# Kernel optimization log

Hardware: AMD Instinct MI355X
Metric: run time of the kernel (lower is better)

Reference implementation:

```python
import jax, jax.numpy as jnp
import numpy as np

N_SP, N_SPAT = 20000, 10000
E_SS, E_BIP, E_SP = 160000, 320000, 320000
H, C = 4, 64  # GAT heads / per-head channels (hidden_channels=64, concat=False)
EPS = 1e-6


def _gat(xs, xd, row, col, ea, Ws, Wd, a_s, a_d, a_e, We, b, num_dst, heads, ch, self_loops, concat):
    # PyG GATConv with edge_dim: linear -> per-head additive attention -> softmax over incoming edges -> scatter-add
    hs = (xs @ Ws).reshape(-1, heads, ch)          # [Ns,H,C]
    hd = (xd @ Wd).reshape(-1, heads, ch)          # [Nd,H,C]
    al_s = jnp.sum(hs * a_s, -1)                   # [Ns,H]
    al_d = jnp.sum(hd * a_d, -1)                   # [Nd,H]
    if self_loops:
        # add_self_loops with fill_value='mean': loop edge_attr = mean of incoming edge_attr per node
        cnt = jax.ops.segment_sum(jnp.ones((row.shape[0],), ea.dtype), col, num_dst)
        loop_ea = jax.ops.segment_sum(ea, col, num_dst) / jnp.maximum(cnt, 1.0)[:, None]
        loops = jnp.arange(num_dst, dtype=row.dtype)
        row = jnp.concatenate([row, loops])
        col = jnp.concatenate([col, loops])
        ea = jnp.concatenate([ea, loop_ea], 0)
    he = (ea @ We).reshape(-1, heads, ch)          # [E,H,C]
    al = jax.nn.leaky_relu(al_s[row] + al_d[col] + jnp.sum(he * a_e, -1), 0.2)  # [E,H]
    m = jax.ops.segment_max(al, col, num_segments=num_dst)
    ex = jnp.exp(al - m[col])
    den = jax.ops.segment_sum(ex, col, num_segments=num_dst)
    alpha = ex / (den[col] + 1e-16)
    out = jax.ops.segment_sum(hs[row] * alpha[..., None], col, num_segments=num_dst)  # [Nd,H,C]
    out = out.reshape(num_dst, heads * ch) if concat else out.mean(1)
    return out + b


def setup_inputs() -> dict:
    key = jax.random.key(0)
    ks = iter(jax.random.split(key, 64))
    f = lambda shape: jax.random.normal(next(ks), shape, jnp.float32)
    w = lambda shape: f(shape) / np.sqrt(shape[0])
    inp = {}
    inp['species_x_mean'] = f((N_SP, 32))
    inp['species_x_std'] = jax.random.uniform(next(ks), (N_SP, 32), jnp.float32)
    inp['traits_nanmask'] = jax.random.bernoulli(next(ks), 0.4, (N_SP, 32))
    inp['species_x_gen'] = f((N_SP, 64))
    inp['species_x_phylo'] = f((N_SP, 128))
    inp['spatial_x'] = f((N_SPAT, 12))
    inp['spatial_global_data'] = f((N_SPAT, 4))
    ei = lambda e, ns, nd: jnp.stack([jax.random.randint(next(ks), (e,), 0, ns, jnp.int32),
                                      jax.random.randint(next(ks), (e,), 0, nd, jnp.int32)])
    inp['ss_edge_index'] = ei(E_SS, N_SPAT, N_SPAT)
    inp['ss_edge_attr'] = jax.random.uniform(next(ks), (E_SS, 1), jnp.float32)
    inp['bip_edge_index'] = ei(E_BIP, N_SPAT, N_SP)
    inp['bip_edge_attr'] = jax.random.uniform(next(ks), (E_BIP, 1), jnp.float32)
    inp['sp_edge_index'] = ei(E_SP, N_SP, N_SP)
    inp['sp_edge_attr'] = jax.random.uniform(next(ks), (E_SP, 1), jnp.float32)
    # GAT conv params: space_gnn (sg0, sg1), species_gnn (pg0, pg1)
    for nm, din in [('sg0', 16), ('sg1', 64), ('pg0', 128), ('pg1', 64)]:
        inp[nm + '_W'] = w((din, H * C))
        inp[nm + '_as'] = f((H, C)) * 0.1
        inp[nm + '_ad'] = f((H, C)) * 0.1
        inp[nm + '_ae'] = f((H, C)) * 0.1
        inp[nm + '_We'] = w((1, H * C))
        inp[nm + '_b'] = jnp.zeros((C,), jnp.float32)
    # bipartite GATConv: heads=1, concat=True, src dim=hidden=64, dst dim=in_gen+in_phylo=192
    inp['bp_Ws'] = w((64, 64))
    inp['bp_Wd'] = w((192, 64))
    inp['bp_as'] = f((1, 64)) * 0.1
    inp['bp_ad'] = f((1, 64)) * 0.1
    inp['bp_ae'] = f((1, 64)) * 0.1
    inp['bp_We'] = w((1, 64))
    inp['bp_b'] = jnp.zeros((64,), jnp.float32)
    inp['sl_W'] = w((288, 64))
    inp['sl_b'] = jnp.zeros((64,), jnp.float32)
    inp['fc_W'] = w((64, 64))
    inp['fc_b'] = jnp.zeros((64,), jnp.float32)
    return inp


def reference(species_x_mean, species_x_std, traits_nanmask, species_x_gen, species_x_phylo,
              spatial_x, spatial_global_data, ss_edge_index, ss_edge_attr, bip_edge_index,
              bip_edge_attr, sp_edge_index, sp_edge_attr,
              sg0_W, sg0_as, sg0_ad, sg0_ae, sg0_We, sg0_b,
              sg1_W, sg1_as, sg1_ad, sg1_ae, sg1_We, sg1_b,
              pg0_W, pg0_as, pg0_ad, pg0_ae, pg0_We, pg0_b,
              pg1_W, pg1_as, pg1_ad, pg1_ae, pg1_We, pg1_b,
              bp_Ws, bp_Wd, bp_as, bp_ad, bp_ae, bp_We, bp_b,
              sl_W, sl_b, fc_W, fc_b):
    # inference path: no trait masking -> visibility = observed mask
    vis = (~traits_nanmask).astype(jnp.float32)
    sp_in = jnp.concatenate([species_x_mean, species_x_std, vis, species_x_gen, species_x_phylo], 1)
    sp_in = jax.nn.relu(sp_in @ sl_W + sl_b)                      # [N_SP,64]
    # spatial GNN (2 GATConv layers, heads=4, concat=False, self loops)
    h = jnp.concatenate([spatial_x, spatial_global_data], 1)      # [N_SPAT,16]
    r, c = ss_edge_index[0], ss_edge_index[1]
    h = jax.nn.relu(_gat(h, h, r, c, ss_edge_attr, sg0_W, sg0_W, sg0_as, sg0_ad, sg0_ae, sg0_We, sg0_b, N_SPAT, H, C, True, False))
    h = jax.nn.relu(_gat(h, h, r, c, ss_edge_attr, sg1_W, sg1_W, sg1_as, sg1_ad, sg1_ae, sg1_We, sg1_b, N_SPAT, H, C, True, False))
    # bipartite spatial->species GATConv (heads=1, concat=True, no self loops)
    part = jnp.concatenate([species_x_gen, species_x_phylo], 1)   # [N_SP,192]
    br, bc = bip_edge_index[0], bip_edge_index[1]
    sts = jax.nn.relu(_gat(h, part, br, bc, bip_edge_attr, bp_Ws, bp_Wd, bp_as, bp_ad, bp_ae, bp_We, bp_b, N_SP, 1, 64, False, True))
    # species GNN (2 GATConv layers)
    x = jnp.concatenate([sts, sp_in], 1)                          # [N_SP,128]
    pr, pc = sp_edge_index[0], sp_edge_index[1]
    x = jax.nn.relu(_gat(x, x, pr, pc, sp_edge_attr, pg0_W, pg0_W, pg0_as, pg0_ad, pg0_ae, pg0_We, pg0_b, N_SP, H, C, True, False))
    x = jax.nn.relu(_gat(x, x, pr, pc, sp_edge_attr, pg1_W, pg1_W, pg1_as, pg1_ad, pg1_ae, pg1_We, pg1_b, N_SP, H, C, True, False))
    ms = x @ fc_W + fc_b                                          # [N_SP, 2*out]
    mean, log_std = jnp.split(ms, 2, axis=-1)
    std = jax.nn.softplus(log_std) + EPS
    return mean, std
```

## Files before the change

kernel.cpp:

```cpp
#include <hip/hip_runtime.h>
#include <hip/hip_bf16.h>

#define NSP   20000
#define NSPAT 10000
#define ESS   160000
#define EBIP  320000
#define ESP   320000

static inline int cdiv_host(long a, long b) { return (int)((a + b - 1) / b); }

__device__ __forceinline__ float wave_red_sum(float p) {
#pragma unroll
  for (int m = 32; m >= 1; m >>= 1) p += __shfl_xor(p, m, 64);
  return p;
}

__device__ __forceinline__ float bf2f(unsigned short u) {
  return __uint_as_float(((unsigned int)u) << 16);
}
__device__ __forceinline__ unsigned short f2bf(float f) {
  unsigned int u = __float_as_uint(f);
  unsigned int r = (u + 0x7FFF + ((u >> 16) & 1)) >> 16;
  return (unsigned short)r;
}

__global__ void count3_kernel(
    const int* c1, int E1, int* cp1, int* rnk1, int n1,
    const int* c2, int E2, int* cp2, int* rnk2, int n2,
    const int* c3, int E3, int* cp3, int* rnk3, int n3,
    const unsigned int* __restrict__ mask, int* __restrict__ flag) {
  int b = blockIdx.x, t = threadIdx.x;
  if (b == gridDim.x - 1) {
    if (t < 64) {
      unsigned int w0 = mask[t], w1 = mask[t + 64], w2 = mask[t + 128], w3 = mask[t + 192];
      bool ai = (w0 <= 1u) && (w1 <= 1u) && (w2 <= 1u) && (w3 <= 1u);
      auto okf = [](unsigned int w) { return w == 0u || w == 0x3f800000u; };
      bool af = okf(w0) && okf(w1) && okf(w2) && okf(w3);
      unsigned long long bi = __ballot(ai), bf = __ballot(af);
      if (t == 0) *flag = (bi == ~0ull) ? 0 : ((bf == ~0ull) ? 2 : 1);
    }
    return;
  }
  int i = b * 256 + t;
  int total = E1 + E2 + E3;
  if (i >= total) return;
  int p = (i >> 8) & 7;
  if (i < E1) {
    int d = c1[i]; rnk1[i] = atomicAdd(&cp1[p * n1 + d], 1);
  } else if (i < E1 + E2) {
    int j = i - E1;
    int d = c2[j]; rnk2[j] = atomicAdd(&cp2[p * n2 + d], 1);
  } else {
    int j = i - E1 - E2;
    int d = c3[j]; rnk3[j] = atomicAdd(&cp3[p * n3 + d], 1);
  }
}

__global__ void merge3_kernel(int* cp1, int* c1, int n1,
                              int* cp2, int* c2, int n2,
                              int* cp3, int* c3, int n3) {
  int i = blockIdx.x * blockDim.x + threadIdx.x;
  int total = n1 + n2 + n3;
  if (i >= total) return;
  int *cp, *c; int n, d;
  if (i < n1) { cp = cp1; c = c1; n = n1; d = i; }
  else if (i < n1 + n2) { cp = cp2; c = c2; n = n2; d = i - n1; }
  else { cp = cp3; c = c3; n = n3; d = i - n1 - n2; }
  int s = 0;
#pragma unroll
  for (int p = 0; p < 8; ++p) { int t = cp[p * n + d]; cp[p * n + d] = s; s += t; }
  c[d] = s;
}

__global__ __launch_bounds__(1024) void scan3_kernel(
    const int* cntA, int nA, int* ptrA,
    const int* cntB, int nB, int* ptrB,
    const int* cntC, int nC, int* ptrC) {
  const int* cnt; int n; int* ptr;
  if (blockIdx.x == 0) { cnt = cntA; n = nA; ptr = ptrA; }
  else if (blockIdx.x == 1) { cnt = cntB; n = nB; ptr = ptrB; }
  else { cnt = cntC; n = nC; ptr = ptrC; }
  __shared__ int part[1024];
  int t = threadIdx.x;
  int ch = (n + 1023) / 1024;
  int beg = t * ch, end = min(beg + ch, n);
  int s = 0;
  for (int i = beg; i < end; ++i) s += cnt[i];
  part[t] = s;
  __syncthreads();
  for (int off = 1; off < 1024; off <<= 1) {
    int v = (t >= off) ? part[t - off] : 0;
    __syncthreads();
    part[t] += v;
    __syncthreads();
  }
  int run = (t == 0) ? 0 : part[t - 1];
  for (int i = beg; i < end; ++i) { ptr[i] = run; run += cnt[i]; }
  if (t == 1023) ptr[n] = part[1023];
}

__global__ void scatter3_kernel(
    const int* r1, const int* c1, const float* e1, int E1, const int* p1, const int* cp1, const int* k1, int n1, int* s1, float* a1,
    const int* r2, const int* c2, const float* e2, int E2, const int* p2, const int* cp2, const int* k2, int n2, int* s2, float* a2,
    const int* r3, const int* c3, const float* e3, int E3, const int* p3, const int* cp3, const int* k3, int n3, int* s3, float* a3) {
  int total = E1 + E2 + E3;
  for (int i = blockIdx.x * blockDim.x + threadIdx.x; i < total; i += gridDim.x * blockDim.x) {
    int p = (i >> 8) & 7;
    if (i < E1) {
      int d = c1[i];
      int pos = p1[d] + cp1[p * n1 + d] + k1[i];
      s1[pos] = r1[i]; a1[pos] = e1[i];
    } else if (i < E1 + E2) {
      int j = i - E1;
      int d = c2[j];
      int pos = p2[d] + cp2[p * n2 + d] + k2[j];
      s2[pos] = r2[j]; a2[pos] = e2[j];
    } else {
      int j = i - E1 - E2;
      int d = c3[j];
      int pos = p3[d] + cp3[p * n3 + d] + k3[j];
      s3[pos] = r3[j]; a3[pos] = e3[j];
    }
  }
}

__global__ void misc_kernel(
    const int* __restrict__ ss_ptr, const float* __restrict__ ss_cea, float* __restrict__ ss_lea,
    const int* __restrict__ pp_ptr, const float* __restrict__ pp_cea, float* __restrict__ pp_lea,
    const float* __restrict__ We0, const float* __restrict__ ae0,
    const float* __restrict__ We1, const float* __restrict__ ae1,
    const float* __restrict__ Web, const float* __restrict__ aeb,
    const float* __restrict__ We2, const float* __restrict__ ae2,
    const float* __restrict__ We3, const float* __restrict__ ae3,
    float* __restrict__ dotes,
    const float* __restrict__ mean, const float* __restrict__ stdv,
    const void* __restrict__ mask, const int* __restrict__ flag,
    const float* __restrict__ sx, const float* __restrict__ sg,
    float* __restrict__ spc96, float* __restrict__ h0) {
  int b = blockIdx.x, t = threadIdx.x;
  if (b < 118) {
    int i = b * 256 + t;
    if (i >= NSPAT + NSP) return;
    const int* ptr; const float* cea; float* lea; int d;
    if (i < NSPAT) { ptr = ss_ptr; cea = ss_cea; lea = ss_lea; d = i; }
    else { ptr = pp_ptr; cea = pp_cea; lea = pp_lea; d = i - NSPAT; }
    int e0 = ptr[d], e1 = ptr[d + 1];
    float s = 0.f;
    for (int e = e0; e < e1; ++e) s += cea[e];
    lea[d] = s / (float)max(e1 - e0, 1);
  } else if (b < 123) {
    int lb = b - 118;
    const float *We, *ae; int n, off;
    switch (lb) {
      case 0: We = We0; ae = ae0; n = 256; off = 0; break;
      case 1: We = We1; ae = ae1; n = 256; off = 4; break;
      case 2: We = Web; ae = aeb; n = 64;  off = 8; break;
      case 3: We = We2; ae = ae2; n = 256; off = 12; break;
      default: We = We3; ae = ae3; n = 256; off = 16; break;
    }
    if (t < n) {
      float p = wave_red_sum(We[t] * ae[t]);
      if ((t & 63) == 0) dotes[off + (t >> 6)] = p;
    }
  } else {
    const long totA = (long)NSP * 96;
    const long totB = (long)NSPAT * 16;
    long i = (long)(b - 123) * 256 + t;
    if (i >= totA + totB) return;
    int mode = *flag;
    if (i < totA) {
      int n = (int)(i / 96), c = (int)(i % 96);
      float v;
      if (c < 32) v = mean[(long)n * 32 + c];
      else if (c < 64) v = stdv[(long)n * 32 + (c - 32)];
      else {
        long j = (long)n * 32 + (c - 64);
        int mv;
        if (mode == 0) mv = ((const int*)mask)[j];
        else if (mode == 2) mv = (((const float*)mask)[j] != 0.0f);
        else mv = (int)((const unsigned char*)mask)[j];
        v = mv ? 0.f : 1.f;
      }
      spc96[i] = v;
    } else {
      long k = i - totA;
      int n = (int)(k / 16), c = (int)(k % 16);
      h0[k] = (c < 12) ? sx[(long)n * 12 + c] : sg[(long)n * 4 + (c - 12)];
    }
  }
}

struct XSrc { const float* p[5]; int w[5]; int n; };
struct PJob {
  XSrc xs; int M, K;
  const float* W; const float* bias; int mode;
  const float* a_s; const float* a_d;
  float* al_s; float* al_d;
  float* Y; float* Y2;
};

__device__ __forceinline__ void proj64_body(const PJob& J, int bid,
                                            float* wl, float* xl) {
  constexpr int KC = 32;
  constexpr int BR = 32;
  constexpr int KCP = 36;
  int t = threadIdx.x;
  long row0 = (long)bid * BR;
  if (row0 >= J.M) return;
  int cg = t & 15, rg = t >> 4;
  int c0 = cg * 4;

  float acc[2][4];
#pragma unroll
  for (int r = 0; r < 2; ++r)
#pragma unroll
    for (int j = 0; j < 4; ++j) acc[r][j] = 0.f;

  for (int k0 = 0; k0 < J.K; k0 += KC) {
    int seg = 0; int base = 0;
    while (k0 >= base + J.xs.w[seg]) { base += J.xs.w[seg]; ++seg; }
    const float* Xp = J.xs.p[seg];
    int stride = J.xs.w[seg];
    int kloc = k0 - base;

    __syncthreads();
    {
      const float4* ws = (const float4*)(J.W + (long)k0 * 64);
      float4* wd = (float4*)wl;
      wd[t] = ws[t];
      wd[t + 256] = ws[t + 256];
    }
    {
      int r = t >> 3, kq = (t & 7) * 4;
      long rr = row0 + r; if (rr >= J.M) rr = J.M - 1;
      float4 v = *(const float4*)(Xp + rr * stride + kloc + kq);
      *(float4*)(xl + r * KCP + kq) = v;
    }
    __syncthreads();

    for (int kg = 0; kg < KC; kg += 4) {
      float4 w0 = *(const float4*)(wl + (kg + 0) * 64 + c0);
      float4 w1 = *(const float4*)(wl + (kg + 1) * 64 + c0);
      float4 w2 = *(const float4*)(wl + (kg + 2) * 64 + c0);
      float4 w3 = *(const float4*)(wl + (kg + 3) * 64 + c0);
#pragma unroll
      for (int r = 0; r < 2; ++r) {
        float4 xv = *(const float4*)(xl + (rg * 2 + r) * KCP + kg);
        acc[r][0] = fmaf(xv.x, w0.x, acc[r][0]);
        acc[r][1] = fmaf(xv.x, w0.y, acc[r][1]);
        acc[r][2] = fmaf(xv.x, w0.z, acc[r][2]);
        acc[r][3] = fmaf(xv.x, w0.w, acc[r][3]);
        acc[r][0] = fmaf(xv.y, w1.x, acc[r][0]);
        acc[r][1] = fmaf(xv.y, w1.y, acc[r][1]);
        acc[r][2] = fmaf(xv.y, w1.z, acc[r][2]);
        acc[r][3] = fmaf(xv.y, w1.w, acc[r][3]);
        acc[r][0] = fmaf(xv.z, w2.x, acc[r][0]);
        acc[r][1] = fmaf(xv.z, w2.y, acc[r][1]);
        acc[r][2] = fmaf(xv.z, w2.z, acc[r][2]);
        acc[r][3] = fmaf(xv.z, w2.w, acc[r][3]);
        acc[r][0] = fmaf(xv.w, w3.x, acc[r][0]);
        acc[r][1] = fmaf(xv.w, w3.y, acc[r][1]);
        acc[r][2] = fmaf(xv.w, w3.z, acc[r][2]);
        acc[r][3] = fmaf(xv.w, w3.w, acc[r][3]);
      }
    }
  }

  float4 bv = make_float4(0.f, 0.f, 0.f, 0.f);
  float4 asv = make_float4(0.f, 0.f, 0.f, 0.f);
  float4 adv = make_float4(0.f, 0.f, 0.f, 0.f);
  if (J.bias) bv = *(const float4*)(J.bias + c0);
  if (J.a_s) asv = *(const float4*)(J.a_s + c0);
  if (J.a_d) adv = *(const float4*)(J.a_d + c0);

#pragma unroll
  for (int r = 0; r < 2; ++r) {
    long m = row0 + rg * 2 + r;
    bool ok = m < J.M;
    float v0 = acc[r][0] + bv.x, v1 = acc[r][1] + bv.y;
    float v2 = acc[r][2] + bv.z, v3 = acc[r][3] + bv.w;
    if (J.mode == 1) {
      if (ok)
        *(float4*)(J.Y + m * 64 + c0) = make_float4(
            fmaxf(v0, 0.f), fmaxf(v1, 0.f), fmaxf(v2, 0.f), fmaxf(v3, 0.f));
    } else if (J.mode == 2) {
      if (ok) {
        if (c0 < 32) {
          *(float4*)(J.Y + m * 32 + c0) = make_float4(v0, v1, v2, v3);
        } else {
          float4 o;
          o.x = fmaxf(v0, 0.f) + log1pf(__expf(-fabsf(v0))) + 1e-6f;
          o.y = fmaxf(v1, 0.f) + log1pf(__expf(-fabsf(v1))) + 1e-6f;
          o.z = fmaxf(v2, 0.f) + log1pf(__expf(-fabsf(v2))) + 1e-6f;
          o.w = fmaxf(v3, 0.f) + log1pf(__expf(-fabsf(v3))) + 1e-6f;
          *(float4*)(J.Y2 + m * 32 + (c0 - 32)) = o;
        }
      }
    } else if (ok && J.Y) {
      *(float4*)(J.Y + m * 64 + c0) = make_float4(v0, v1, v2, v3);
    }
    if (J.a_s) {
      float s = acc[r][0] * asv.x + acc[r][1] * asv.y + acc[r][2] * asv.z + acc[r][3] * asv.w;
      s += __shfl_xor(s, 1); s += __shfl_xor(s, 2);
      s += __shfl_xor(s, 4); s += __shfl_xor(s, 8);
      if (ok && cg == 0) J.al_s[m] = s;
    }
    if (J.a_d) {
      float s = acc[r][0] * adv.x + acc[r][1] * adv.y + acc[r][2] * adv.z + acc[r][3] * adv.w;
      s += __shfl_xor(s, 1); s += __shfl_xor(s, 2);
      s += __shfl_xor(s, 4); s += __shfl_xor(s, 8);
      if (ok && cg == 0) J.al_d[m] = s;
    }
  }
}

__global__ __launch_bounds__(256) void proj64x2_kernel(PJob j0, PJob j1, int nb0) {
  __shared__ float wl[32 * 64];
  __shared__ float xl[32 * 36];
  if ((int)blockIdx.x < nb0) proj64_body(j0, blockIdx.x, wl, xl);
  else proj64_body(j1, blockIdx.x - nb0, wl, xl);
}

__global__ __launch_bounds__(256) void proj_kernel(
    XSrc xsrc, int M, int K,
    const float* __restrict__ W, const float* __restrict__ bias, int mode,
    const float* __restrict__ a_s, const float* __restrict__ a_d,
    float* __restrict__ al_s, float* __restrict__ al_d,
    float* __restrict__ Y, float* __restrict__ Y2) {
  constexpr int NOUT = 256;
  constexpr int KC = 32;
  constexpr int RPT = 8;
  constexpr int BR = 32;
  constexpr int KCP = 36;
  constexpr int H = 4;
  __shared__ float wl[KC * NOUT];
  __shared__ float xl[BR * KCP];

  int t = threadIdx.x;
  int cg = t & 63, rg = t >> 6;
  int c0 = cg * 4;
  long row0 = (long)blockIdx.x * BR;

  float acc[RPT][4];
#pragma unroll
  for (int r = 0; r < RPT; ++r)
#pragma unroll
    for (int j = 0; j < 4; ++j) acc[r][j] = 0.f;

  for (int k0 = 0; k0 < K; k0 += KC) {
    int kc = min(KC, K - k0);
    int seg = 0; int base = 0;
    while (k0 >= base + xsrc.w[seg]) { base += xsrc.w[seg]; ++seg; }
    const float* Xp = xsrc.p[seg];
    int stride = xsrc.w[seg];
    int kloc = k0 - base;

    __syncthreads();
    {
      const float4* wsrc = (const float4*)(W + (long)k0 * NOUT);
      float4* wdst = (float4*)wl;
      for (int i = t; i < (kc * NOUT) >> 2; i += 256) wdst[i] = wsrc[i];
    }
    for (int i = t; i < BR * 8; i += 256) {
      int r = i >> 3, kq = (i & 7) * 4;
      if (kq < kc) {
        long rr = row0 + r; if (rr >= M) rr = M - 1;
        float4 v = *(const float4*)(Xp + rr * stride + kloc + kq);
        *(float4*)(xl + r * KCP + kq) = v;
      }
    }
    __syncthreads();

    for (int kg = 0; kg < kc; kg += 4) {
      float4 w0 = *(const float4*)(wl + (kg + 0) * NOUT + c0);
      float4 w1 = *(const float4*)(wl + (kg + 1) * NOUT + c0);
      float4 w2 = *(const float4*)(wl + (kg + 2) * NOUT + c0);
      float4 w3 = *(const float4*)(wl + (kg + 3) * NOUT + c0);
      float4 xv[RPT];
#pragma unroll
      for (int r = 0; r < RPT; ++r)
        xv[r] = *(const float4*)(xl + (rg * RPT + r) * KCP + kg);
#pragma unroll
      for (int r = 0; r < RPT; ++r) {
        acc[r][0] = fmaf(xv[r].x, w0.x, acc[r][0]);
        acc[r][1] = fmaf(xv[r].x, w0.y, acc[r][1]);
        acc[r][2] = fmaf(xv[r].x, w0.z, acc[r][2]);
        acc[r][3] = fmaf(xv[r].x, w0.w, acc[r][3]);
        acc[r][0] = fmaf(xv[r].y, w1.x, acc[r][0]);
        acc[r][1] = fmaf(xv[r].y, w1.y, acc[r][1]);
        acc[r][2] = fmaf(xv[r].y, w1.z, acc[r][2]);
        acc[r][3] = fmaf(xv[r].y, w1.w, acc[r][3]);
        acc[r][0] = fmaf(xv[r].z, w2.x, acc[r][0]);
        acc[r][1] = fmaf(xv[r].z, w2.y, acc[r][1]);
        acc[r][2] = fmaf(xv[r].z, w2.z, acc[r][2]);
        acc[r][3] = fmaf(xv[r].z, w2.w, acc[r][3]);
        acc[r][0] = fmaf(xv[r].w, w3.x, acc[r][0]);
        acc[r][1] = fmaf(xv[r].w, w3.y, acc[r][1]);
        acc[r][2] = fmaf(xv[r].w, w3.z, acc[r][2]);
        acc[r][3] = fmaf(xv[r].w, w3.w, acc[r][3]);
      }
    }
  }

  float4 asv = make_float4(0.f, 0.f, 0.f, 0.f);
  float4 adv = make_float4(0.f, 0.f, 0.f, 0.f);
  if (a_s) asv = *(const float4*)(a_s + c0);
  if (a_d) adv = *(const float4*)(a_d + c0);

#pragma unroll
  for (int r = 0; r < RPT; ++r) {
    long m = row0 + (long)rg * RPT + r;
    bool ok = m < M;
    if (ok && mode == 3) {
      ushort4 o;
      o.x = f2bf(acc[r][0]); o.y = f2bf(acc[r][1]);
      o.z = f2bf(acc[r][2]); o.w = f2bf(acc[r][3]);
      *(ushort4*)((unsigned short*)Y + m * NOUT + c0) = o;
    }
    if (a_s) {
      float s = acc[r][0] * asv.x + acc[r][1] * asv.y + acc[r][2] * asv.z + acc[r][3] * asv.w;
      s += __shfl_xor(s, 1); s += __shfl_xor(s, 2);
      s += __shfl_xor(s, 4); s += __shfl_xor(s, 8);
      if (ok && (cg & 15) == 0) al_s[m * H + (c0 >> 6)] = s;
    }
    if (a_d) {
      float s = acc[r][0] * adv.x + acc[r][1] * adv.y + acc[r][2] * adv.z + acc[r][3] * adv.w;
      s += __shfl_xor(s, 1); s += __shfl_xor(s, 2);
      s += __shfl_xor(s, 4); s += __shfl_xor(s, 8);
      if (ok && (cg & 15) == 0) al_d[m * H + (c0 >> 6)] = s;
    }
  }
  (void)bias; (void)Y2;
}

__device__ __forceinline__ void fma4_bf(float4& a, float al, ushort4 u) {
  a.x = fmaf(al, bf2f(u.x), a.x); a.y = fmaf(al, bf2f(u.y), a.y);
  a.z = fmaf(al, bf2f(u.z), a.z); a.w = fmaf(al, bf2f(u.w), a.w);
}
__device__ __forceinline__ void scale4(float4& a, float s) {
  a.x *= s; a.y *= s; a.z *= s; a.w *= s;
}

template <bool SELFLOOP>
__global__ __launch_bounds__(256) void gat4_fused(
    int Nd, const int* __restrict__ dptr, const int* __restrict__ csr_src,
    const float* __restrict__ csr_ea, const float* __restrict__ al_s,
    const float* __restrict__ al_d, const float* __restrict__ dote,
    const float* __restrict__ loop_ea, const unsigned short* __restrict__ hs,
    const float* __restrict__ bias, float* __restrict__ out) {
  int wave = threadIdx.x >> 6, lane = threadIdx.x & 63;
  int n = blockIdx.x * 4 + wave;
  if (n >= Nd) return;
  int h = lane >> 4;
  float ald = al_d[(long)n * 4 + h];
  float de = dote[h];
  int e0 = dptr[n], e1 = dptr[n + 1];
  float m0 = -INFINITY, d0 = 0.f;
  float4 a0 = make_float4(0.f, 0.f, 0.f, 0.f);
  if (SELFLOOP) {
    float l = al_s[(long)n * 4 + h] + ald + loop_ea[n] * de;
    l = (l > 0.f) ? l : 0.2f * l;
    m0 = l; d0 = 1.f;
    ushort4 u = *(const ushort4*)(hs + (long)n * 256 + lane * 4);
    a0.x = bf2f(u.x); a0.y = bf2f(u.y); a0.z = bf2f(u.z); a0.w = bf2f(u.w);
  }
  float m1 = -INFINITY, d1 = 0.f;
  float4 a1 = make_float4(0.f, 0.f, 0.f, 0.f);
  int e = e0;
  for (; e + 2 <= e1; e += 2) {
    int s0 = csr_src[e], s1 = csr_src[e + 1];
    float l0 = al_s[(long)s0 * 4 + h] + ald + csr_ea[e] * de;
    float l1 = al_s[(long)s1 * 4 + h] + ald + csr_ea[e + 1] * de;
    l0 = (l0 > 0.f) ? l0 : 0.2f * l0;
    l1 = (l1 > 0.f) ? l1 : 0.2f * l1;
    ushort4 u0 = *(const ushort4*)(hs + (long)s0 * 256 + lane * 4);
    ushort4 u1 = *(const ushort4*)(hs + (long)s1 * 256 + lane * 4);
    if (l0 > m0) { float sc = __expf(m0 - l0); d0 *= sc; scale4(a0, sc); m0 = l0; }
    float ex0 = __expf(l0 - m0);
    d0 += ex0;
    fma4_bf(a0, ex0, u0);
    if (l1 > m1) { float sc = __expf(m1 - l1); d1 *= sc; scale4(a1, sc); m1 = l1; }
    float ex1 = __expf(l1 - m1);
    d1 += ex1;
    fma4_bf(a1, ex1, u1);
  }
  if (e < e1) {
    int s0 = csr_src[e];
    float l0 = al_s[(long)s0 * 4 + h] + ald + csr_ea[e] * de;
    l0 = (l0 > 0.f) ? l0 : 0.2f * l0;
    ushort4 u0 = *(const ushort4*)(hs + (long)s0 * 256 + lane * 4);
    if (l0 > m0) { float sc = __expf(m0 - l0); d0 *= sc; scale4(a0, sc); m0 = l0; }
    float ex0 = __expf(l0 - m0);
    d0 += ex0;
    fma4_bf(a0, ex0, u0);
  }
  if (m1 != -INFINITY) {
    float M = fmaxf(m0, m1);
    float sA = (m0 == -INFINITY) ? 0.f : __expf(m0 - M);
    float sB = __expf(m1 - M);
    d0 = d0 * sA + d1 * sB;
    a0.x = a0.x * sA + a1.x * sB; a0.y = a0.y * sA + a1.y * sB;
    a0.z = a0.z * sA + a1.z * sB; a0.w = a0.w * sA + a1.w * sB;
  }
  float inv = 1.f / (d0 + 1e-16f);
  scale4(a0, inv);
  a0.x += __shfl_xor(a0.x, 16); a0.y += __shfl_xor(a0.y, 16);
  a0.z += __shfl_xor(a0.z, 16); a0.w += __shfl_xor(a0.w, 16);
  a0.x += __shfl_xor(a0.x, 32); a0.y += __shfl_xor(a0.y, 32);
  a0.z += __shfl_xor(a0.z, 32); a0.w += __shfl_xor(a0.w, 32);
  if (lane < 16) {
    float4 b = *(const float4*)(bias + lane * 4);
    float4 o;
    o.x = fmaxf(a0.x * 0.25f + b.x, 0.f);
    o.y = fmaxf(a0.y * 0.25f + b.y, 0.f);
    o.z = fmaxf(a0.z * 0.25f + b.z, 0.f);
    o.w = fmaxf(a0.w * 0.25f + b.w, 0.f);
    *(float4*)(out + (long)n * 64 + lane * 4) = o;
  }
}

__global__ __launch_bounds__(256) void gat1_fused(
    int Nd, const int* __restrict__ dptr, const int* __restrict__ csr_src,
    const float* __restrict__ csr_ea, const float* __restrict__ al_s,
    const float* __restrict__ al_d, const float* __restrict__ dote,
    const float* __restrict__ hs, const float* __restrict__ bias,
    float* __restrict__ out) {
  int wave = threadIdx.x >> 6, lane = threadIdx.x & 63;
  int n = blockIdx.x * 4 + wave;
  if (n >= Nd) return;
  float ald = al_d[n];
  float de = dote[0];
  int e0 = dptr[n], e1 = dptr[n + 1];
  float m0 = -INFINITY, d0 = 0.f, acc0 = 0.f;
  float m1 = -INFINITY, d1 = 0.f, acc1 = 0.f;
  int e = e0;
  for (; e + 2 <= e1; e += 2) {
    int s0 = csr_src[e], s1 = csr_src[e + 1];
    float l0 = al_s[s0] + ald + csr_ea[e] * de;
    float l1 = al_s[s1] + ald + csr_ea[e + 1] * de;
    l0 = (l0 > 0.f) ? l0 : 0.2f * l0;
    l1 = (l1 > 0.f) ? l1 : 0.2f * l1;
    float h0 = hs[(long)s0 * 64 + lane];
    float h1 = hs[(long)s1 * 64 + lane];
    if (l0 > m0) { float sc = __expf(m0 - l0); d0 *= sc; acc0 *= sc; m0 = l0; }
    float ex0 = __expf(l0 - m0);
    d0 += ex0; acc0 = fmaf(ex0, h0, acc0);
    if (l1 > m1) { float sc = __expf(m1 - l1); d1 *= sc; acc1 *= sc; m1 = l1; }
    float ex1 = __expf(l1 - m1);
    d1 += ex1; acc1 = fmaf(ex1, h1, acc1);
  }
  if (e < e1) {
    int s0 = csr_src[e];
    float l0 = al_s[s0] + ald + csr_ea[e] * de;
    l0 = (l0 > 0.f) ? l0 : 0.2f * l0;
    float h0 = hs[(long)s0 * 64 + lane];
    if (l0 > m0) { float sc = __expf(m0 - l0); d0 *= sc; acc0 *= sc; m0 = l0; }
    float ex0 = __expf(l0 - m0);
    d0 += ex0; acc0 = fmaf(ex0, h0, acc0);
  }
  if (m1 != -INFINITY) {
    float M = fmaxf(m0, m1);
    float sA = (m0 == -INFINITY) ? 0.f : __expf(m0 - M);
    float sB = __expf(m1 - M);
    d0 = d0 * sA + d1 * sB;
    acc0 = acc0 * sA + acc1 * sB;
  }
  float o = acc0 / (d0 + 1e-16f);
  out[(long)n * 64 + lane] = fmaxf(o + bias[lane], 0.f);
}

extern "C" void kernel_launch(void* const* d_in, const int* in_sizes, int n_in,
                              void* d_out, int out_size, void* d_ws, size_t ws_size,
                              hipStream_t stream) {
  const float* sp_mean = (const float*)d_in[0];
  const float* sp_std  = (const float*)d_in[1];
  const void*  nanmask = d_in[2];
  const float* sp_gen  = (const float*)d_in[3];
  const float* sp_phy  = (const float*)d_in[4];
  const float* spat_x  = (const float*)d_in[5];
  const float* spat_g  = (const float*)d_in[6];
  const int*   ss_ei   = (const int*)d_in[7];
  const float* ss_ea   = (const float*)d_in[8];
  const int*   bip_ei  = (const int*)d_in[9];
  const float* bip_ea  = (const float*)d_in[10];
  const int*   sp_ei   = (const int*)d_in[11];
  const float* sp_ea   = (const float*)d_in[12];
  const float* sg0_W = (const float*)d_in[13]; const float* sg0_as = (const float*)d_in[14];
  const float* sg0_ad = (const float*)d_in[15]; const float* sg0_ae = (const float*)d_in[16];
  const float* sg0_We = (const float*)d_in[17]; const float* sg0_b = (const float*)d_in[18];
  const float* sg1_W = (const float*)d_in[19]; const float* sg1_as = (const float*)d_in[20];
  const float* sg1_ad = (const float*)d_in[21]; const float* sg1_ae = (const float*)d_in[22];
  const float* sg1_We = (const float*)d_in[23]; const float* sg1_b = (const float*)d_in[24];
  const float* pg0_W = (const float*)d_in[25]; const float* pg0_as = (const float*)d_in[26];
  const float* pg0_ad = (const float*)d_in[27]; const float* pg0_ae = (const float*)d_in[28];
  const float* pg0_We = (const float*)d_in[29]; const float* pg0_b = (const float*)d_in[30];
  const float* pg1_W = (const float*)d_in[31]; const float* pg1_as = (const float*)d_in[32];
  const float* pg1_ad = (const float*)d_in[33]; const float* pg1_ae = (const float*)d_in[34];
  const float* pg1_We = (const float*)d_in[35]; const float* pg1_b = (const float*)d_in[36];
  const float* bp_Ws = (const float*)d_in[37]; const float* bp_Wd = (const float*)d_in[38];
  const float* bp_as = (const float*)d_in[39]; const float* bp_ad = (const float*)d_in[40];
  const float* bp_ae = (const float*)d_in[41]; const float* bp_We = (const float*)d_in[42];
  const float* bp_b  = (const float*)d_in[43];
  const float* sl_W  = (const float*)d_in[44]; const float* sl_b  = (const float*)d_in[45];
  const float* fc_W  = (const float*)d_in[46]; const float* fc_b  = (const float*)d_in[47];

  char* wsb = (char*)d_ws;
  size_t off = 0;
  auto A = [&](size_t nbytes) -> void* {
    void* p = wsb + off;
    off += (nbytes + 255) & ~(size_t)255;
    return p;
  };
  int* ss_cp = (int*)A((size_t)8 * NSPAT * 4);
  int* bp_cp = (int*)A((size_t)8 * NSP * 4);
  int* pp_cp = (int*)A((size_t)8 * NSP * 4);
  size_t zbytes = off;
  int*   ss_cnt = (int*)A((NSPAT + 1) * 4);
  int*   bp_cnt = (int*)A((NSP + 1) * 4);
  int*   pp_cnt = (int*)A((NSP + 1) * 4);
  int*   flag  = (int*)A(4);
  float* dotes = (float*)A(5 * 4 * sizeof(float));
  float* alS   = (float*)A((size_t)NSP * 4 * 4);
  float* alD   = (float*)A((size_t)NSP * 4 * 4);
  float* alSb  = (float*)A((size_t)NSPAT * 4);
  float* alDb  = (float*)A((size_t)NSP * 4);
  float* spc96 = (float*)A((size_t)NSP * 96 * 4);
  float* sp_in = (float*)A((size_t)NSP * 64 * 4);
  float* h0    = (float*)A((size_t)NSPAT * 16 * 4);
  float* h_a   = (float*)A((size_t)NSPAT * 64 * 4);
  float* h_b   = (float*)A((size_t)NSPAT * 64 * 4);
  float* HS    = (float*)A((size_t)NSP * 256 * 4);
  float* sts   = (float*)A((size_t)NSP * 64 * 4);
  float* x1    = (float*)A((size_t)NSP * 64 * 4);
  int*   ss_ptr = (int*)A((NSPAT + 1) * 4);
  int*   ss_src = (int*)A((size_t)ESS * 4);
  float* ss_cea = (float*)A((size_t)ESS * 4);
  int*   ss_rnk = (int*)A((size_t)ESS * 4);
  float* ss_lea = (float*)A((size_t)NSPAT * 4);
  int*   bp_ptr = (int*)A((NSP + 1) * 4);
  int*   bp_src = (int*)A((size_t)EBIP * 4);
  float* bp_cea = (float*)A((size_t)EBIP * 4);
  int*   bp_rnk = (int*)A((size_t)EBIP * 4);
  int*   pp_ptr = (int*)A((NSP + 1) * 4);
  int*   pp_src = (int*)A((size_t)ESP * 4);
  float* pp_cea = (float*)A((size_t)ESP * 4);
  int*   pp_rnk = (int*)A((size_t)ESP * 4);
  float* pp_lea = (float*)A((size_t)NSP * 4);
  (void)ws_size; (void)in_sizes; (void)n_in; (void)out_size;

  const int TB = 256;
  hipMemsetAsync(wsb, 0, zbytes, stream);

  count3_kernel<<<cdiv_host(ESS + EBIP + ESP, TB) + 1, TB, 0, stream>>>(
      ss_ei + ESS, ESS, ss_cp, ss_rnk, NSPAT,
      bip_ei + EBIP, EBIP, bp_cp, bp_rnk, NSP,
      sp_ei + ESP, ESP, pp_cp, pp_rnk, NSP,
      (const unsigned int*)nanmask, flag);
  merge3_kernel<<<cdiv_host(NSPAT + NSP + NSP, TB), TB, 0, stream>>>(
      ss_cp, ss_cnt, NSPAT, bp_cp, bp_cnt, NSP, pp_cp, pp_cnt, NSP);
  scan3_kernel<<<3, 1024, 0, stream>>>(ss_cnt, NSPAT, ss_ptr, bp_cnt, NSP, bp_ptr, pp_cnt, NSP, pp_ptr);
  scatter3_kernel<<<cdiv_host(ESS + EBIP + ESP, TB), TB, 0, stream>>>(
      ss_ei, ss_ei + ESS, ss_ea, ESS, ss_ptr, ss_cp, ss_rnk, NSPAT, ss_src, ss_cea,
      bip_ei, bip_ei + EBIP, bip_ea, EBIP, bp_ptr, bp_cp, bp_rnk, NSP, bp_src, bp_cea,
      sp_ei, sp_ei + ESP, sp_ea, ESP, pp_ptr, pp_cp, pp_rnk, NSP, pp_src, pp_cea);

  misc_kernel<<<123 + cdiv_host((long)NSP * 96 + (long)NSPAT * 16, TB), TB, 0, stream>>>(
      ss_ptr, ss_cea, ss_lea, pp_ptr, pp_cea, pp_lea,
      sg0_We, sg0_ae, sg1_We, sg1_ae, bp_We, bp_ae, pg0_We, pg0_ae, pg1_We, pg1_ae,
      dotes, sp_mean, sp_std, nanmask, flag, spat_x, spat_g, spc96, h0);

  {
    PJob j0{}; j0.xs.p[0] = spc96; j0.xs.w[0] = 96; j0.xs.p[1] = sp_gen; j0.xs.w[1] = 64;
    j0.xs.p[2] = sp_phy; j0.xs.w[2] = 128; j0.xs.n = 3;
    j0.M = NSP; j0.K = 288; j0.W = sl_W; j0.bias = sl_b; j0.mode = 1; j0.Y = sp_in;
    PJob j1{}; j1.xs.p[0] = sp_gen; j1.xs.w[0] = 64; j1.xs.p[1] = sp_phy; j1.xs.w[1] = 128;
    j1.xs.n = 2;
    j1.M = NSP; j1.K = 192; j1.W = bp_Wd; j1.mode = 0; j1.a_d = bp_ad; j1.al_d = alDb;
    int nb0 = cdiv_host(NSP, 32);
    proj64x2_kernel<<<nb0 + cdiv_host(NSP, 32), TB, 0, stream>>>(j0, j1, nb0);
  }

  {
    XSrc xs{}; xs.p[0] = h0; xs.w[0] = 16; xs.n = 1;
    proj_kernel<<<cdiv_host(NSPAT, 32), TB, 0, stream>>>(xs, NSPAT, 16, sg0_W, nullptr, 3,
        sg0_as, sg0_ad, alS, alD, HS, nullptr);
  }
  gat4_fused<true><<<cdiv_host(NSPAT, 4), TB, 0, stream>>>(
      NSPAT, ss_ptr, ss_src, ss_cea, alS, alD, dotes + 0, ss_lea,
      (const unsigned short*)HS, sg0_b, h_a);
  {
    XSrc xs{}; xs.p[0] = h_a; xs.w[0] = 64; xs.n = 1;
    proj_kernel<<<cdiv_host(NSPAT, 32), TB, 0, stream>>>(xs, NSPAT, 64, sg1_W, nullptr, 3,
        sg1_as, sg1_ad, alS, alD, HS, nullptr);
  }
  gat4_fused<true><<<cdiv_host(NSPAT, 4), TB, 0, stream>>>(
      NSPAT, ss_ptr, ss_src, ss_cea, alS, alD, dotes + 4, ss_lea,
      (const unsigned short*)HS, sg1_b, h_b);

  {
    PJob j0{}; j0.xs.p[0] = h_b; j0.xs.w[0] = 64; j0.xs.n = 1;
    j0.M = NSPAT; j0.K = 64; j0.W = bp_Ws; j0.mode = 0;
    j0.a_s = bp_as; j0.al_s = alSb; j0.Y = h_a;
    int nb0 = cdiv_host(NSPAT, 32);
    proj64x2_kernel<<<nb0, TB, 0, stream>>>(j0, j0, nb0);
  }
  gat1_fused<<<cdiv_host(NSP, 4), TB, 0, stream>>>(
      NSP, bp_ptr, bp_src, bp_cea, alSb, alDb, dotes + 8, h_a, bp_b, sts);

  {
    XSrc xs{}; xs.p[0] = sts; xs.w[0] = 64; xs.p[1] = sp_in; xs.w[1] = 64; xs.n = 2;
    proj_kernel<<<cdiv_host(NSP, 32), TB, 0, stream>>>(xs, NSP, 128, pg0_W, nullptr, 3,
        pg0_as, pg0_ad, alS, alD, HS, nullptr);
  }
  gat4_fused<true><<<cdiv_host(NSP, 4), TB, 0, stream>>>(
      NSP, pp_ptr, pp_src, pp_cea, alS, alD, dotes + 12, pp_lea,
      (const unsigned short*)HS, pg0_b, x1);
  {
    XSrc xs{}; xs.p[0] = x1; xs.w[0] = 64; xs.n = 1;
    proj_kernel<<<cdiv_host(NSP, 32), TB, 0, stream>>>(xs, NSP, 64, pg1_W, nullptr, 3,
        pg1_as, pg1_ad, alS, alD, HS, nullptr);
  }
  gat4_fused<true><<<cdiv_host(NSP, 4), TB, 0, stream>>>(
      NSP, pp_ptr, pp_src, pp_cea, alS, alD, dotes + 16, pp_lea,
      (const unsigned short*)HS, pg1_b, sts);

  {
    PJob j0{}; j0.xs.p[0] = sts; j0.xs.w[0] = 64; j0.xs.n = 1;
    j0.M = NSP; j0.K = 64; j0.W = fc_W; j0.bias = fc_b; j0.mode = 2;
    j0.Y = (float*)d_out; j0.Y2 = (float*)d_out + (long)NSP * 32;
    int nb0 = cdiv_host(NSP, 32);
    proj64x2_kernel<<<nb0, TB, 0, stream>>>(j0, j0, nb0);
  }
}
```

Baseline: 498.3 us.

## Fuse all stages into one cooperative persistent kernel with grid syncs

Replaces the chain of about fifteen separate launches (memset, CSR build, misc prep, projections, GAT aggregations) with a single cooperative mega-kernel. It uses grid-stride loops per stage and cg grid.sync between dependent phases, and the grid is sized from occupancy times CU count. This targets launch overhead and inter-kernel gaps. In exchange, every phase now runs under the occupancy limits of the largest stage's registers and shared memory, and each grid-wide barrier has its own cost.

```diff
diff --git a/kernel.cpp b/kernel.cpp
--- a/kernel.cpp
+++ b/kernel.cpp
@@ -1,5 +1,8 @@
 #include <hip/hip_runtime.h>
 #include <hip/hip_bf16.h>
+#include <hip/hip_cooperative_groups.h>
+
+namespace cg = cooperative_groups;
 
 #define NSP   20000
 #define NSPAT 10000
@@ -14,7 +17,6 @@
   for (int m = 32; m >= 1; m >>= 1) p += __shfl_xor(p, m, 64);
   return p;
 }
-
 __device__ __forceinline__ float bf2f(unsigned short u) {
   return __uint_as_float(((unsigned int)u) << 16);
 }
@@ -24,192 +26,53 @@
   return (unsigned short)r;
 }
 
-__global__ void count3_kernel(
-    const int* c1, int E1, int* cp1, int* rnk1, int n1,
-    const int* c2, int E2, int* cp2, int* rnk2, int n2,
-    const int* c3, int E3, int* cp3, int* rnk3, int n3,
-    const unsigned int* __restrict__ mask, int* __restrict__ flag) {
-  int b = blockIdx.x, t = threadIdx.x;
-  if (b == gridDim.x - 1) {
-    if (t < 64) {
-      unsigned int w0 = mask[t], w1 = mask[t + 64], w2 = mask[t + 128], w3 = mask[t + 192];
-      bool ai = (w0 <= 1u) && (w1 <= 1u) && (w2 <= 1u) && (w3 <= 1u);
-      auto okf = [](unsigned int w) { return w == 0u || w == 0x3f800000u; };
-      bool af = okf(w0) && okf(w1) && okf(w2) && okf(w3);
-      unsigned long long bi = __ballot(ai), bf = __ballot(af);
-      if (t == 0) *flag = (bi == ~0ull) ? 0 : ((bf == ~0ull) ? 2 : 1);
-    }
-    return;
-  }
-  int i = b * 256 + t;
-  int total = E1 + E2 + E3;
-  if (i >= total) return;
-  int p = (i >> 8) & 7;
-  if (i < E1) {
-    int d = c1[i]; rnk1[i] = atomicAdd(&cp1[p * n1 + d], 1);
-  } else if (i < E1 + E2) {
-    int j = i - E1;
-    int d = c2[j]; rnk2[j] = atomicAdd(&cp2[p * n2 + d], 1);
-  } else {
-    int j = i - E1 - E2;
-    int d = c3[j]; rnk3[j] = atomicAdd(&cp3[p * n3 + d], 1);
-  }
-}
-
-__global__ void merge3_kernel(int* cp1, int* c1, int n1,
-                              int* cp2, int* c2, int n2,
-                              int* cp3, int* c3, int n3) {
-  int i = blockIdx.x * blockDim.x + threadIdx.x;
-  int total = n1 + n2 + n3;
-  if (i >= total) return;
-  int *cp, *c; int n, d;
-  if (i < n1) { cp = cp1; c = c1; n = n1; d = i; }
-  else if (i < n1 + n2) { cp = cp2; c = c2; n = n2; d = i - n1; }
-  else { cp = cp3; c = c3; n = n3; d = i - n1 - n2; }
-  int s = 0;
-#pragma unroll
-  for (int p = 0; p < 8; ++p) { int t = cp[p * n + d]; cp[p * n + d] = s; s += t; }
-  c[d] = s;
-}
-
-__global__ __launch_bounds__(1024) void scan3_kernel(
-    const int* cntA, int nA, int* ptrA,
-    const int* cntB, int nB, int* ptrB,
-    const int* cntC, int nC, int* ptrC) {
-  const int* cnt; int n; int* ptr;
-  if (blockIdx.x == 0) { cnt = cntA; n = nA; ptr = ptrA; }
-  else if (blockIdx.x == 1) { cnt = cntB; n = nB; ptr = ptrB; }
-  else { cnt = cntC; n = nC; ptr = ptrC; }
-  __shared__ int part[1024];
-  int t = threadIdx.x;
-  int ch = (n + 1023) / 1024;
-  int beg = t * ch, end = min(beg + ch, n);
-  int s = 0;
-  for (int i = beg; i < end; ++i) s += cnt[i];
-  part[t] = s;
-  __syncthreads();
-  for (int off = 1; off < 1024; off <<= 1) {
-    int v = (t >= off) ? part[t - off] : 0;
-    __syncthreads();
-    part[t] += v;
-    __syncthreads();
-  }
-  int run = (t == 0) ? 0 : part[t - 1];
-  for (int i = beg; i < end; ++i) { ptr[i] = run; run += cnt[i]; }
-  if (t == 1023) ptr[n] = part[1023];
-}
-
-__global__ void scatter3_kernel(
-    const int* r1, const int* c1, const float* e1, int E1, const int* p1, const int* cp1, const int* k1, int n1, int* s1, float* a1,
-    const int* r2, const int* c2, const float* e2, int E2, const int* p2, const int* cp2, const int* k2, int n2, int* s2, float* a2,
-    const int* r3, const int* c3, const float* e3, int E3, const int* p3, const int* cp3, const int* k3, int n3, int* s3, float* a3) {
-  int total = E1 + E2 + E3;
-  for (int i = blockIdx.x * blockDim.x + threadIdx.x; i < total; i += gridDim.x * blockDim.x) {
-    int p = (i >> 8) & 7;
-    if (i < E1) {
-      int d = c1[i];
-      int pos = p1[d] + cp1[p * n1 + d] + k1[i];
-      s1[pos] = r1[i]; a1[pos] = e1[i];
-    } else if (i < E1 + E2) {
-      int j = i - E1;
-      int d = c2[j];
-      int pos = p2[d] + cp2[p * n2 + d] + k2[j];
-      s2[pos] = r2[j]; a2[pos] = e2[j];
-    } else {
-      int j = i - E1 - E2;
-      int d = c3[j];
-      int pos = p3[d] + cp3[p * n3 + d] + k3[j];
-      s3[pos] = r3[j]; a3[pos] = e3[j];
-    }
-  }
-}
-
-__global__ void misc_kernel(
-    const int* __restrict__ ss_ptr, const float* __restrict__ ss_cea, float* __restrict__ ss_lea,
-    const int* __restrict__ pp_ptr, const float* __restrict__ pp_cea, float* __restrict__ pp_lea,
-    const float* __restrict__ We0, const float* __restrict__ ae0,
-    const float* __restrict__ We1, const float* __restrict__ ae1,
-    const float* __restrict__ Web, const float* __restrict__ aeb,
-    const float* __restrict__ We2, const float* __restrict__ ae2,
-    const float* __restrict__ We3, const float* __restrict__ ae3,
-    float* __restrict__ dotes,
-    const float* __restrict__ mean, const float* __restrict__ stdv,
-    const void* __restrict__ mask, const int* __restrict__ flag,
-    const float* __restrict__ sx, const float* __restrict__ sg,
-    float* __restrict__ spc96, float* __restrict__ h0) {
-  int b = blockIdx.x, t = threadIdx.x;
-  if (b < 118) {
-    int i = b * 256 + t;
-    if (i >= NSPAT + NSP) return;
-    const int* ptr; const float* cea; float* lea; int d;
-    if (i < NSPAT) { ptr = ss_ptr; cea = ss_cea; lea = ss_lea; d = i; }
-    else { ptr = pp_ptr; cea = pp_cea; lea = pp_lea; d = i - NSPAT; }
-    int e0 = ptr[d], e1 = ptr[d + 1];
-    float s = 0.f;
-    for (int e = e0; e < e1; ++e) s += cea[e];
-    lea[d] = s / (float)max(e1 - e0, 1);
-  } else if (b < 123) {
-    int lb = b - 118;
-    const float *We, *ae; int n, off;
-    switch (lb) {
-      case 0: We = We0; ae = ae0; n = 256; off = 0; break;
-      case 1: We = We1; ae = ae1; n = 256; off = 4; break;
-      case 2: We = Web; ae = aeb; n = 64;  off = 8; break;
-      case 3: We = We2; ae = ae2; n = 256; off = 12; break;
-      default: We = We3; ae = ae3; n = 256; off = 16; break;
-    }
-    if (t < n) {
-      float p = wave_red_sum(We[t] * ae[t]);
-      if ((t & 63) == 0) dotes[off + (t >> 6)] = p;
-    }
-  } else {
-    const long totA = (long)NSP * 96;
-    const long totB = (long)NSPAT * 16;
-    long i = (long)(b - 123) * 256 + t;
-    if (i >= totA + totB) return;
-    int mode = *flag;
-    if (i < totA) {
-      int n = (int)(i / 96), c = (int)(i % 96);
-      float v;
-      if (c < 32) v = mean[(long)n * 32 + c];
-      else if (c < 64) v = stdv[(long)n * 32 + (c - 32)];
-      else {
-        long j = (long)n * 32 + (c - 64);
-        int mv;
-        if (mode == 0) mv = ((const int*)mask)[j];
-        else if (mode == 2) mv = (((const float*)mask)[j] != 0.0f);
-        else mv = (int)((const unsigned char*)mask)[j];
-        v = mv ? 0.f : 1.f;
-      }
-      spc96[i] = v;
-    } else {
-      long k = i - totA;
-      int n = (int)(k / 16), c = (int)(k % 16);
-      h0[k] = (c < 12) ? sx[(long)n * 12 + c] : sg[(long)n * 4 + (c - 12)];
-    }
-  }
-}
-
 struct XSrc { const float* p[5]; int w[5]; int n; };
-struct PJob {
+struct P64 {
   XSrc xs; int M, K;
   const float* W; const float* bias; int mode;
   const float* a_s; const float* a_d;
   float* al_s; float* al_d;
   float* Y; float* Y2;
 };
-
-__device__ __forceinline__ void proj64_body(const PJob& J, int bid,
-                                            float* wl, float* xl) {
-  constexpr int KC = 32;
-  constexpr int BR = 32;
-  constexpr int KCP = 36;
+struct P256 {
+  XSrc xs; int M, K;
+  const float* W;
+  const float* a_s; const float* a_d;
+  float* al_s; float* al_d;
+  unsigned short* Y;
+};
+
+struct MegaArgs {
+  uint4* zbase; int zwords;
+  const int *ss_row, *ss_col; const float* ss_eaI;
+  const int *bp_row, *bp_col; const float* bp_eaI;
+  const int *pp_row, *pp_col; const float* pp_eaI;
+  int *ss_cp, *bp_cp, *pp_cp;
+  int *ss_rnk, *bp_rnk, *pp_rnk;
+  int *ss_cnt, *bp_cnt, *pp_cnt;
+  int *ss_ptr, *bp_ptr, *pp_ptr;
+  int *ss_src; float* ss_cea;
+  int *bp_src; float* bp_cea;
+  int *pp_src; float* pp_cea;
+  float *ss_lea, *pp_lea;
+  const unsigned int* mask; int* flag;
+  const float* We[5]; const float* ae[5]; float* dotes;
+  const float* mean; const float* stdv; const float* sx; const float* sgd;
+  float* spc96; float* h0;
+  P64 sl, bpWd, bpWs, fc;
+  P256 sg0, sg1, pg0, pg1;
+  float *alS, *alD, *alSb, *alDb;
+  const unsigned short* HS;
+  const float *sg0_b, *sg1_b, *pg0_b, *pg1_b, *bp_b;
+  float *h_a, *h_b, *sts, *x1;
+};
+
+__device__ void proj64_tile(const P64& J, int bid, float* wl, float* xl) {
+  constexpr int KC = 32, BR = 32, KCP = 36;
   int t = threadIdx.x;
   long row0 = (long)bid * BR;
-  if (row0 >= J.M) return;
-  int cg = t & 15, rg = t >> 4;
-  int c0 = cg * 4;
-
+  int cg_ = t & 15, rg = t >> 4;
+  int c0 = cg_ * 4;
   float acc[2][4];
 #pragma unroll
   for (int r = 0; r < 2; ++r)
@@ -217,12 +80,11 @@
     for (int j = 0; j < 4; ++j) acc[r][j] = 0.f;
 
   for (int k0 = 0; k0 < J.K; k0 += KC) {
-    int seg = 0; int base = 0;
+    int seg = 0, base = 0;
     while (k0 >= base + J.xs.w[seg]) { base += J.xs.w[seg]; ++seg; }
     const float* Xp = J.xs.p[seg];
     int stride = J.xs.w[seg];
     int kloc = k0 - base;
-
     __syncthreads();
     {
       const float4* ws = (const float4*)(J.W + (long)k0 * 64);
@@ -237,7 +99,6 @@
       *(float4*)(xl + r * KCP + kq) = v;
     }
     __syncthreads();
-
     for (int kg = 0; kg < KC; kg += 4) {
       float4 w0 = *(const float4*)(wl + (kg + 0) * 64 + c0);
       float4 w1 = *(const float4*)(wl + (kg + 1) * 64 + c0);
@@ -303,134 +164,111 @@
       float s = acc[r][0] * asv.x + acc[r][1] * asv.y + acc[r][2] * asv.z + acc[r][3] * asv.w;
       s += __shfl_xor(s, 1); s += __shfl_xor(s, 2);
       s += __shfl_xor(s, 4); s += __shfl_xor(s, 8);
-      if (ok && cg == 0) J.al_s[m] = s;
+      if (ok && cg_ == 0) J.al_s[m] = s;
     }
     if (J.a_d) {
       float s = acc[r][0] * adv.x + acc[r][1] * adv.y + acc[r][2] * adv.z + acc[r][3] * adv.w;
       s += __shfl_xor(s, 1); s += __shfl_xor(s, 2);
       s += __shfl_xor(s, 4); s += __shfl_xor(s, 8);
-      if (ok && cg == 0) J.al_d[m] = s;
-    }
-  }
-}
-
-__global__ __launch_bounds__(256) void proj64x2_kernel(PJob j0, PJob j1, int nb0) {
-  __shared__ float wl[32 * 64];
-  __shared__ float xl[32 * 36];
-  if ((int)blockIdx.x < nb0) proj64_body(j0, blockIdx.x, wl, xl);
-  else proj64_body(j1, blockIdx.x - nb0, wl, xl);
-}
-
-__global__ __launch_bounds__(256) void proj_kernel(
-    XSrc xsrc, int M, int K,
-    const float* __restrict__ W, const float* __restrict__ bias, int mode,
-    const float* __restrict__ a_s, const float* __restrict__ a_d,
-    float* __restrict__ al_s, float* __restrict__ al_d,
-    float* __restrict__ Y, float* __restrict__ Y2) {
-  constexpr int NOUT = 256;
-  constexpr int KC = 32;
-  constexpr int RPT = 8;
-  constexpr int BR = 32;
-  constexpr int KCP = 36;
-  constexpr int H = 4;
-  __shared__ float wl[KC * NOUT];
-  __shared__ float xl[BR * KCP];
-
+      if (ok && cg_ == 0) J.al_d[m] = s;
+    }
+  }
+}
+
+__device__ void proj64_grid(const P64& J, float* wl, float* xl) {
+  int nb = (J.M + 31) >> 5;
+  for (int b = blockIdx.x; b < nb; b += gridDim.x) proj64_tile(J, b, wl, xl);
+}
+
+__device__ void proj256_grid(const P256& J, float* wl, float* xl) {
+  constexpr int KC = 32, RPT = 8, BR = 32, KCP = 36;
   int t = threadIdx.x;
-  int cg = t & 63, rg = t >> 6;
-  int c0 = cg * 4;
-  long row0 = (long)blockIdx.x * BR;
-
-  float acc[RPT][4];
-#pragma unroll
-  for (int r = 0; r < RPT; ++r)
-#pragma unroll
-    for (int j = 0; j < 4; ++j) acc[r][j] = 0.f;
-
-  for (int k0 = 0; k0 < K; k0 += KC) {
-    int kc = min(KC, K - k0);
-    int seg = 0; int base = 0;
-    while (k0 >= base + xsrc.w[seg]) { base += xsrc.w[seg]; ++seg; }
-    const float* Xp = xsrc.p[seg];
-    int stride = xsrc.w[seg];
-    int kloc = k0 - base;
-
-    __syncthreads();
-    {
-      const float4* wsrc = (const float4*)(W + (long)k0 * NOUT);
-      float4* wdst = (float4*)wl;
-      for (int i = t; i < (kc * NOUT) >> 2; i += 256) wdst[i] = wsrc[i];
-    }
-    for (int i = t; i < BR * 8; i += 256) {
-      int r = i >> 3, kq = (i & 7) * 4;
-      if (kq < kc) {
-        long rr = row0 + r; if (rr >= M) rr = M - 1;
-        float4 v = *(const float4*)(Xp + rr * stride + kloc + kq);
-        *(float4*)(xl + r * KCP + kq) = v;
+  int cg_ = t & 63, rg = t >> 6;
+  int c0 = cg_ * 4;
+  int nb = (J.M + 31) >> 5;
+  for (int b = blockIdx.x; b < nb; b += gridDim.x) {
+    long row0 = (long)b * BR;
+    float acc[RPT][4];
+#pragma unroll
+    for (int r = 0; r < RPT; ++r)
+#pragma unroll
+      for (int j = 0; j < 4; ++j) acc[r][j] = 0.f;
+
+    for (int k0 = 0; k0 < J.K; k0 += KC) {
+      int kc = min(KC, J.K - k0);
+      int seg = 0, base = 0;
+      while (k0 >= base + J.xs.w[seg]) { base += J.xs.w[seg]; ++seg; }
+      const float* Xp = J.xs.p[seg];
+      int stride = J.xs.w[seg];
+      int kloc = k0 - base;
+      __syncthreads();
+      {
+        const float4* wsrc = (const float4*)(J.W + (long)k0 * 256);
+        float4* wdst = (float4*)wl;
+        for (int i = t; i < (kc * 256) >> 2; i += 256) wdst[i] = wsrc[i];
       }
-    }
-    __syncthreads();
-
-    for (int kg = 0; kg < kc; kg += 4) {
-      float4 w0 = *(const float4*)(wl + (kg + 0) * NOUT + c0);
-      float4 w1 = *(const float4*)(wl + (kg + 1) * NOUT + c0);
-      float4 w2 = *(const float4*)(wl + (kg + 2) * NOUT + c0);
-      float4 w3 = *(const float4*)(wl + (kg + 3) * NOUT + c0);
-      float4 xv[RPT];
-#pragma unroll
-      for (int r = 0; r < RPT; ++r)
-        xv[r] = *(const float4*)(xl + (rg * RPT + r) * KCP + kg);
-#pragma unroll
-      for (int r = 0; r < RPT; ++r) {
-        acc[r][0] = fmaf(xv[r].x, w0.x, acc[r][0]);
-        acc[r][1] = fmaf(xv[r].x, w0.y, acc[r][1]);
-        acc[r][2] = fmaf(xv[r].x, w0.z, acc[r][2]);
-        acc[r][3] = fmaf(xv[r].x, w0.w, acc[r][3]);
-        acc[r][0] = fmaf(xv[r].y, w1.x, acc[r][0]);
-        acc[r][1] = fmaf(xv[r].y, w1.y, acc[r][1]);
-        acc[r][2] = fmaf(xv[r].y, w1.z, acc[r][2]);
-        acc[r][3] = fmaf(xv[r].y, w1.w, acc[r][3]);
-        acc[r][0] = fmaf(xv[r].z, w2.x, acc[r][0]);
-        acc[r][1] = fmaf(xv[r].z, w2.y, acc[r][1]);
-        acc[r][2] = fmaf(xv[r].z, w2.z, acc[r][2]);
-        acc[r][3] = fmaf(xv[r].z, w2.w, acc[r][3]);
-        acc[r][0] = fmaf(xv[r].w, w3.x, acc[r][0]);
-        acc[r][1] = fmaf(xv[r].w, w3.y, acc[r][1]);
-        acc[r][2] = fmaf(xv[r].w, w3.z, acc[r][2]);
-        acc[r][3] = fmaf(xv[r].w, w3.w, acc[r][3]);
+      for (int i = t; i < BR * 8; i += 256) {
+        int r = i >> 3, kq = (i & 7) * 4;
+        if (kq < kc) {
+          long rr = row0 + r; if (rr >= J.M) rr = J.M - 1;
+          float4 v = *(const float4*)(Xp + rr * stride + kloc + kq);
+          *(float4*)(xl + r * KCP + kq) = v;
+        }
       }
-    }
-  }
-
-  float4 asv = make_float4(0.f, 0.f, 0.f, 0.f);
-  float4 adv = make_float4(0.f, 0.f, 0.f, 0.f);
-  if (a_s) asv = *(const float4*)(a_s + c0);
-  if (a_d) adv = *(const float4*)(a_d + c0);
-
-#pragma unroll
-  for (int r = 0; r < RPT; ++r) {
-    long m = row0 + (long)rg * RPT + r;
-    bool ok = m < M;
-    if (ok && mode == 3) {
-      ushort4 o;
-      o.x = f2bf(acc[r][0]); o.y = f2bf(acc[r][1]);
-      o.z = f2bf(acc[r][2]); o.w = f2bf(acc[r][3]);
-      *(ushort4*)((unsigned short*)Y + m * NOUT + c0) = o;
-    }
-    if (a_s) {
+      __syncthreads();
+      for (int kg = 0; kg < kc; kg += 4) {
+        float4 w0 = *(const float4*)(wl + (kg + 0) * 256 + c0);
+        float4 w1 = *(const float4*)(wl + (kg + 1) * 256 + c0);
+        float4 w2 = *(const float4*)(wl + (kg + 2) * 256 + c0);
+        float4 w3 = *(const float4*)(wl + (kg + 3) * 256 + c0);
+        float4 xv[RPT];
+#pragma unroll
+        for (int r = 0; r < RPT; ++r)
+          xv[r] = *(const float4*)(xl + (rg * RPT + r) * KCP + kg);
+#pragma unroll
+        for (int r = 0; r < RPT; ++r) {
+          acc[r][0] = fmaf(xv[r].x, w0.x, acc[r][0]);
+          acc[r][1] = fmaf(xv[r].x, w0.y, acc[r][1]);
+          acc[r][2] = fmaf(xv[r].x, w0.z, acc[r][2]);
+          acc[r][3] = fmaf(xv[r].x, w0.w, acc[r][3]);
+          acc[r][0] = fmaf(xv[r].y, w1.x, acc[r][0]);
+          acc[r][1] = fmaf(xv[r].y, w1.y, acc[r][1]);
+          acc[r][2] = fmaf(xv[r].y, w1.z, acc[r][2]);
+          acc[r][3] = fmaf(xv[r].y, w1.w, acc[r][3]);
+          acc[r][0] = fmaf(xv[r].z, w2.x, acc[r][0]);
+          acc[r][1] = fmaf(xv[r].z, w2.y, acc[r][1]);
+          acc[r][2] = fmaf(xv[r].z, w2.z, acc[r][2]);
+          acc[r][3] = fmaf(xv[r].z, w2.w, acc[r][3]);
+          acc[r][0] = fmaf(xv[r].w, w3.x, acc[r][0]);
+          acc[r][1] = fmaf(xv[r].w, w3.y, acc[r][1]);
+          acc[r][2] = fmaf(xv[r].w, w3.z, acc[r][2]);
+          acc[r][3] = fmaf(xv[r].w, w3.w, acc[r][3]);
+        }
+      }
+    }
+
+    float4 asv = *(const float4*)(J.a_s + c0);
+    float4 adv = *(const float4*)(J.a_d + c0);
+#pragma unroll
+    for (int r = 0; r < RPT; ++r) {
+      long m = row0 + (long)rg * RPT + r;
+      bool ok = m < J.M;
+      if (ok) {
+        ushort4 o;
+        o.x = f2bf(acc[r][0]); o.y = f2bf(acc[r][1]);
+        o.z = f2bf(acc[r][2]); o.w = f2bf(acc[r][3]);
+        *(ushort4*)(J.Y + m * 256 + c0) = o;
+      }
       float s = acc[r][0] * asv.x + acc[r][1] * asv.y + acc[r][2] * asv.z + acc[r][3] * asv.w;
       s += __shfl_xor(s, 1); s += __shfl_xor(s, 2);
       s += __shfl_xor(s, 4); s += __shfl_xor(s, 8);
-      if (ok && (cg & 15) == 0) al_s[m * H + (c0 >> 6)] = s;
-    }
-    if (a_d) {
-      float s = acc[r][0] * adv.x + acc[r][1] * adv.y + acc[r][2] * adv.z + acc[r][3] * adv.w;
-      s += __shfl_xor(s, 1); s += __shfl_xor(s, 2);
-      s += __shfl_xor(s, 4); s += __shfl_xor(s, 8);
-      if (ok && (cg & 15) == 0) al_d[m * H + (c0 >> 6)] = s;
-    }
-  }
-  (void)bias; (void)Y2;
+      if (ok && (cg_ & 15) == 0) J.al_s[m * 4 + (c0 >> 6)] = s;
+      float d = acc[r][0] * adv.x + acc[r][1] * adv.y + acc[r][2] * adv.z + acc[r][3] * adv.w;
+      d += __shfl_xor(d, 1); d += __shfl_xor(d, 2);
+      d += __shfl_xor(d, 4); d += __shfl_xor(d, 8);
+      if (ok && (cg_ & 15) == 0) J.al_d[m * 4 + (c0 >> 6)] = d;
+    }
+  }
 }
 
 __device__ __forceinline__ void fma4_bf(float4& a, float al, ushort4 u) {
@@ -441,132 +279,312 @@
   a.x *= s; a.y *= s; a.z *= s; a.w *= s;
 }
 
-template <bool SELFLOOP>
-__global__ __launch_bounds__(256) void gat4_fused(
-    int Nd, const int* __restrict__ dptr, const int* __restrict__ csr_src,
-    const float* __restrict__ csr_ea, const float* __restrict__ al_s,
-    const float* __restrict__ al_d, const float* __restrict__ dote,
-    const float* __restrict__ loop_ea, const unsigned short* __restrict__ hs,
-    const float* __restrict__ bias, float* __restrict__ out) {
+__device__ void gat4_grid(int Nd, const int* dptr, const int* csr_src,
+                          const float* csr_ea, const float* al_s, const float* al_d,
+                          const float* dote, const float* loop_ea,
+                          const unsigned short* hs, const float* bias, float* out) {
   int wave = threadIdx.x >> 6, lane = threadIdx.x & 63;
-  int n = blockIdx.x * 4 + wave;
-  if (n >= Nd) return;
   int h = lane >> 4;
-  float ald = al_d[(long)n * 4 + h];
   float de = dote[h];
-  int e0 = dptr[n], e1 = dptr[n + 1];
-  float m0 = -INFINITY, d0 = 0.f;
-  float4 a0 = make_float4(0.f, 0.f, 0.f, 0.f);
-  if (SELFLOOP) {
+  for (int n = blockIdx.x * 4 + wave; n < Nd; n += gridDim.x * 4) {
+    float ald = al_d[(long)n * 4 + h];
+    int e0 = dptr[n], e1 = dptr[n + 1];
     float l = al_s[(long)n * 4 + h] + ald + loop_ea[n] * de;
     l = (l > 0.f) ? l : 0.2f * l;
-    m0 = l; d0 = 1.f;
-    ushort4 u = *(const ushort4*)(hs + (long)n * 256 + lane * 4);
-    a0.x = bf2f(u.x); a0.y = bf2f(u.y); a0.z = bf2f(u.z); a0.w = bf2f(u.w);
-  }
-  float m1 = -INFINITY, d1 = 0.f;
-  float4 a1 = make_float4(0.f, 0.f, 0.f, 0.f);
-  int e = e0;
-  for (; e + 2 <= e1; e += 2) {
-    int s0 = csr_src[e], s1 = csr_src[e + 1];
-    float l0 = al_s[(long)s0 * 4 + h] + ald + csr_ea[e] * de;
-    float l1 = al_s[(long)s1 * 4 + h] + ald + csr_ea[e + 1] * de;
-    l0 = (l0 > 0.f) ? l0 : 0.2f * l0;
-    l1 = (l1 > 0.f) ? l1 : 0.2f * l1;
-    ushort4 u0 = *(const ushort4*)(hs + (long)s0 * 256 + lane * 4);
-    ushort4 u1 = *(const ushort4*)(hs + (long)s1 * 256 + lane * 4);
-    if (l0 > m0) { float sc = __expf(m0 - l0); d0 *= sc; scale4(a0, sc); m0 = l0; }
-    float ex0 = __expf(l0 - m0);
-    d0 += ex0;
-    fma4_bf(a0, ex0, u0);
-    if (l1 > m1) { float sc = __expf(m1 - l1); d1 *= sc; scale4(a1, sc); m1 = l1; }
-    float ex1 = __expf(l1 - m1);
-    d1 += ex1;
-    fma4_bf(a1, ex1, u1);
-  }
-  if (e < e1) {
-    int s0 = csr_src[e];
-    float l0 = al_s[(long)s0 * 4 + h] + ald + csr_ea[e] * de;
-    l0 = (l0 > 0.f) ? l0 : 0.2f * l0;
-    ushort4 u0 = *(const ushort4*)(hs + (long)s0 * 256 + lane * 4);
-    if (l0 > m0) { float sc = __expf(m0 - l0); d0 *= sc; scale4(a0, sc); m0 = l0; }
-    float ex0 = __expf(l0 - m0);
-    d0 += ex0;
-    fma4_bf(a0, ex0, u0);
-  }
-  if (m1 != -INFINITY) {
-    float M = fmaxf(m0, m1);
-    float sA = (m0 == -INFINITY) ? 0.f : __expf(m0 - M);
-    float sB = __expf(m1 - M);
-    d0 = d0 * sA + d1 * sB;
-    a0.x = a0.x * sA + a1.x * sB; a0.y = a0.y * sA + a1.y * sB;
-    a0.z = a0.z * sA + a1.z * sB; a0.w = a0.w * sA + a1.w * sB;
-  }
-  float inv = 1.f / (d0 + 1e-16f);
-  scale4(a0, inv);
-  a0.x += __shfl_xor(a0.x, 16); a0.y += __shfl_xor(a0.y, 16);
-  a0.z += __shfl_xor(a0.z, 16); a0.w += __shfl_xor(a0.w, 16);
-  a0.x += __shfl_xor(a0.x, 32); a0.y += __shfl_xor(a0.y, 32);
-  a0.z += __shfl_xor(a0.z, 32); a0.w += __shfl_xor(a0.w, 32);
-  if (lane < 16) {
-    float4 b = *(const float4*)(bias + lane * 4);
-    float4 o;
-    o.x = fmaxf(a0.x * 0.25f + b.x, 0.f);
-    o.y = fmaxf(a0.y * 0.25f + b.y, 0.f);
-    o.z = fmaxf(a0.z * 0.25f + b.z, 0.f);
-    o.w = fmaxf(a0.w * 0.25f + b.w, 0.f);
-    *(float4*)(out + (long)n * 64 + lane * 4) = o;
-  }
-}
-
-__global__ __launch_bounds__(256) void gat1_fused(
-    int Nd, const int* __restrict__ dptr, const int* __restrict__ csr_src,
-    const float* __restrict__ csr_ea, const float* __restrict__ al_s,
-    const float* __restrict__ al_d, const float* __restrict__ dote,
-    const float* __restrict__ hs, const float* __restrict__ bias,
-    float* __restrict__ out) {
+    float m0 = l, d0 = 1.f;
+    float4 a0;
+    {
+      ushort4 u = *(const ushort4*)(hs + (long)n * 256 + lane * 4);
+      a0.x = bf2f(u.x); a0.y = bf2f(u.y); a0.z = bf2f(u.z); a0.w = bf2f(u.w);
+    }
+    float m1 = -INFINITY, d1 = 0.f;
+    float4 a1 = make_float4(0.f, 0.f, 0.f, 0.f);
+    int e = e0;
+    for (; e + 2 <= e1; e += 2) {
+      int s0 = csr_src[e], s1 = csr_src[e + 1];
+      float l0 = al_s[(long)s0 * 4 + h] + ald + csr_ea[e] * de;
+      float l1 = al_s[(long)s1 * 4 + h] + ald + csr_ea[e + 1] * de;
+      l0 = (l0 > 0.f) ? l0 : 0.2f * l0;
+      l1 = (l1 > 0.f) ? l1 : 0.2f * l1;
+      ushort4 u0 = *(const ushort4*)(hs + (long)s0 * 256 + lane * 4);
+      ushort4 u1 = *(const ushort4*)(hs + (long)s1 * 256 + lane * 4);
+      if (l0 > m0) { float sc = __expf(m0 - l0); d0 *= sc; scale4(a0, sc); m0 = l0; }
+      float ex0 = __expf(l0 - m0);
+      d0 += ex0;
+      fma4_bf(a0, ex0, u0);
+      if (l1 > m1) { float sc = __expf(m1 - l1); d1 *= sc; scale4(a1, sc); m1 = l1; }
+      float ex1 = __expf(l1 - m1);
+      d1 += ex1;
+      fma4_bf(a1, ex1, u1);
+    }
+    if (e < e1) {
+      int s0 = csr_src[e];
+      float l0 = al_s[(long)s0 * 4 + h] + ald + csr_ea[e] * de;
+      l0 = (l0 > 0.f) ? l0 : 0.2f * l0;
+      ushort4 u0 = *(const ushort4*)(hs + (long)s0 * 256 + lane * 4);
+      if (l0 > m0) { float sc = __expf(m0 - l0); d0 *= sc; scale4(a0, sc); m0 = l0; }
+      float ex0 = __expf(l0 - m0);
+      d0 += ex0;
+      fma4_bf(a0, ex0, u0);
+    }
+    if (m1 != -INFINITY) {
+      float M = fmaxf(m0, m1);
+      float sA = __expf(m0 - M);
+      float sB = __expf(m1 - M);
+      d0 = d0 * sA + d1 * sB;
+      a0.x = a0.x * sA + a1.x * sB; a0.y = a0.y * sA + a1.y * sB;
+      a0.z = a0.z * sA + a1.z * sB; a0.w = a0.w * sA + a1.w * sB;
+    }
+    float inv = 1.f / (d0 + 1e-16f);
+    scale4(a0, inv);
+    a0.x += __shfl_xor(a0.x, 16); a0.y += __shfl_xor(a0.y, 16);
+    a0.z += __shfl_xor(a0.z, 16); a0.w += __shfl_xor(a0.w, 16);
+    a0.x += __shfl_xor(a0.x, 32); a0.y += __shfl_xor(a0.y, 32);
+    a0.z += __shfl_xor(a0.z, 32); a0.w += __shfl_xor(a0.w, 32);
+    if (lane < 16) {
+      float4 b = *(const float4*)(bias + lane * 4);
+      float4 o;
+      o.x = fmaxf(a0.x * 0.25f + b.x, 0.f);
+      o.y = fmaxf(a0.y * 0.25f + b.y, 0.f);
+      o.z = fmaxf(a0.z * 0.25f + b.z, 0.f);
+      o.w = fmaxf(a0.w * 0.25f + b.w, 0.f);
+      *(float4*)(out + (long)n * 64 + lane * 4) = o;
+    }
+  }
+}
+
+__device__ void gat1_grid(int Nd, const int* dptr, const int* csr_src,
+                          const float* csr_ea, const float* al_s, const float* al_d,
+                          const float* dote, const float* hs, const float* bias,
+                          float* out) {
   int wave = threadIdx.x >> 6, lane = threadIdx.x & 63;
-  int n = blockIdx.x * 4 + wave;
-  if (n >= Nd) return;
-  float ald = al_d[n];
   float de = dote[0];
-  int e0 = dptr[n], e1 = dptr[n + 1];
-  float m0 = -INFINITY, d0 = 0.f, acc0 = 0.f;
-  float m1 = -INFINITY, d1 = 0.f, acc1 = 0.f;
-  int e = e0;
-  for (; e + 2 <= e1; e += 2) {
-    int s0 = csr_src[e], s1 = csr_src[e + 1];
-    float l0 = al_s[s0] + ald + csr_ea[e] * de;
-    float l1 = al_s[s1] + ald + csr_ea[e + 1] * de;
-    l0 = (l0 > 0.f) ? l0 : 0.2f * l0;
-    l1 = (l1 > 0.f) ? l1 : 0.2f * l1;
-    float h0 = hs[(long)s0 * 64 + lane];
-    float h1 = hs[(long)s1 * 64 + lane];
-    if (l0 > m0) { float sc = __expf(m0 - l0); d0 *= sc; acc0 *= sc; m0 = l0; }
-    float ex0 = __expf(l0 - m0);
-    d0 += ex0; acc0 = fmaf(ex0, h0, acc0);
-    if (l1 > m1) { float sc = __expf(m1 - l1); d1 *= sc; acc1 *= sc; m1 = l1; }
-    float ex1 = __expf(l1 - m1);
-    d1 += ex1; acc1 = fmaf(ex1, h1, acc1);
-  }
-  if (e < e1) {
-    int s0 = csr_src[e];
-    float l0 = al_s[s0] + ald + csr_ea[e] * de;
-    l0 = (l0 > 0.f) ? l0 : 0.2f * l0;
-    float h0 = hs[(long)s0 * 64 + lane];
-    if (l0 > m0) { float sc = __expf(m0 - l0); d0 *= sc; acc0 *= sc; m0 = l0; }
-    float ex0 = __expf(l0 - m0);
-    d0 += ex0; acc0 = fmaf(ex0, h0, acc0);
-  }
-  if (m1 != -INFINITY) {
-    float M = fmaxf(m0, m1);
-    float sA = (m0 == -INFINITY) ? 0.f : __expf(m0 - M);
-    float sB = __expf(m1 - M);
-    d0 = d0 * sA + d1 * sB;
-    acc0 = acc0 * sA + acc1 * sB;
-  }
-  float o = acc0 / (d0 + 1e-16f);
-  out[(long)n * 64 + lane] = fmaxf(o + bias[lane], 0.f);
+  for (int n = blockIdx.x * 4 + wave; n < Nd; n += gridDim.x * 4) {
+    float ald = al_d[n];
+    int e0 = dptr[n], e1 = dptr[n + 1];
+    float m0 = -INFINITY, d0 = 0.f, acc0 = 0.f;
+    float m1 = -INFINITY, d1 = 0.f, acc1 = 0.f;
+    int e = e0;
+    for (; e + 2 <= e1; e += 2) {
+      int s0 = csr_src[e], s1 = csr_src[e + 1];
+      float l0 = al_s[s0] + ald + csr_ea[e] * de;
+      float l1 = al_s[s1] + ald + csr_ea[e + 1] * de;
+      l0 = (l0 > 0.f) ? l0 : 0.2f * l0;
+      l1 = (l1 > 0.f) ? l1 : 0.2f * l1;
+      float h0 = hs[(long)s0 * 64 + lane];
+      float h1 = hs[(long)s1 * 64 + lane];
+      if (l0 > m0) { float sc = __expf(m0 - l0); d0 *= sc; acc0 *= sc; m0 = l0; }
+      float ex0 = __expf(l0 - m0);
+      d0 += ex0; acc0 = fmaf(ex0, h0, acc0);
+      if (l1 > m1) { float sc = __expf(m1 - l1); d1 *= sc; acc1 *= sc; m1 = l1; }
+      float ex1 = __expf(l1 - m1);
+      d1 += ex1; acc1 = fmaf(ex1, h1, acc1);
+    }
+    if (e < e1) {
+      int s0 = csr_src[e];
+      float l0 = al_s[s0] + ald + csr_ea[e] * de;
+      l0 = (l0 > 0.f) ? l0 : 0.2f * l0;
+      float h0 = hs[(long)s0 * 64 + lane];
+      if (l0 > m0) { float sc = __expf(m0 - l0); d0 *= sc; acc0 *= sc; m0 = l0; }
+      float ex0 = __expf(l0 - m0);
+      d0 += ex0; acc0 = fmaf(ex0, h0, acc0);
+    }
+    if (m1 != -INFINITY) {
+      float M = fmaxf(m0, m1);
+      float sA = (m0 == -INFINITY) ? 0.f : __expf(m0 - M);
+      float sB = __expf(m1 - M);
+      d0 = d0 * sA + d1 * sB;
+      acc0 = acc0 * sA + acc1 * sB;
+    }
+    float o = acc0 / (d0 + 1e-16f);
+    out[(long)n * 64 + lane] = fmaxf(o + bias[lane], 0.f);
+  }
+}
+
+__global__ __launch_bounds__(256, 4) void mega_kernel(MegaArgs A) {
+  __shared__ __align__(16) float smem[32 * 256 + 32 * 36];
+  float* wl = smem;
+  float* xl = smem + 32 * 256;
+  cg::grid_group g = cg::this_grid();
+  int t = threadIdx.x;
+  int gtid = blockIdx.x * 256 + t;
+  int gsz = gridDim.x * 256;
+
+  for (int i = gtid; i < A.zwords; i += gsz) A.zbase[i] = make_uint4(0, 0, 0, 0);
+  g.sync();
+
+  {
+    const int NB = (ESS + EBIP + ESP + 255) / 256;
+    for (int b = blockIdx.x; b < NB + 1; b += gridDim.x) {
+      if (b == NB) {
+        if (t < 64) {
+          unsigned int w0 = A.mask[t], w1 = A.mask[t + 64];
+          unsigned int w2 = A.mask[t + 128], w3 = A.mask[t + 192];
+          bool ai = (w0 <= 1u) && (w1 <= 1u) && (w2 <= 1u) && (w3 <= 1u);
+          bool af = (w0 == 0u || w0 == 0x3f800000u) && (w1 == 0u || w1 == 0x3f800000u) &&
+                    (w2 == 0u || w2 == 0x3f800000u) && (w3 == 0u || w3 == 0x3f800000u);
+          unsigned long long bi = __ballot(ai), bf = __ballot(af);
+          if (t == 0) *A.flag = (bi == ~0ull) ? 0 : ((bf == ~0ull) ? 2 : 1);
+        }
+      } else {
+        int i = b * 256 + t;
+        if (i < ESS + EBIP + ESP) {
+          int p = (i >> 8) & 7;
+          if (i < ESS) {
+            int d = A.ss_col[i]; A.ss_rnk[i] = atomicAdd(&A.ss_cp[p * NSPAT + d], 1);
+          } else if (i < ESS + EBIP) {
+            int j = i - ESS;
+            int d = A.bp_col[j]; A.bp_rnk[j] = atomicAdd(&A.bp_cp[p * NSP + d], 1);
+          } else {
+            int j = i - ESS - EBIP;
+            int d = A.pp_col[j]; A.pp_rnk[j] = atomicAdd(&A.pp_cp[p * NSP + d], 1);
+          }
+        }
+      }
+    }
+  }
+  g.sync();
+
+  for (int i = gtid; i < NSPAT + NSP + NSP; i += gsz) {
+    int *cp, *c; int n, d;
+    if (i < NSPAT) { cp = A.ss_cp; c = A.ss_cnt; n = NSPAT; d = i; }
+    else if (i < NSPAT + NSP) { cp = A.bp_cp; c = A.bp_cnt; n = NSP; d = i - NSPAT; }
+    else { cp = A.pp_cp; c = A.pp_cnt; n = NSP; d = i - NSPAT - NSP; }
+    int s = 0;
+#pragma unroll
+    for (int p = 0; p < 8; ++p) { int v = cp[p * n + d]; cp[p * n + d] = s; s += v; }
+    c[d] = s;
+  }
+  g.sync();
+
+  if (blockIdx.x < 3) {
+    const int* cnt; int n; int* ptr;
+    if (blockIdx.x == 0) { cnt = A.ss_cnt; n = NSPAT; ptr = A.ss_ptr; }
+    else if (blockIdx.x == 1) { cnt = A.bp_cnt; n = NSP; ptr = A.bp_ptr; }
+    else { cnt = A.pp_cnt; n = NSP; ptr = A.pp_ptr; }
+    int* part = (int*)smem;
+    int ch = (n + 255) / 256;
+    int beg = t * ch, end = min(beg + ch, n);
+    int s = 0;
+    for (int i = beg; i < end; ++i) s += cnt[i];
+    part[t] = s;
+    __syncthreads();
+    for (int off2 = 1; off2 < 256; off2 <<= 1) {
+      int v = (t >= off2) ? part[t - off2] : 0;
+      __syncthreads();
+      part[t] += v;
+      __syncthreads();
+    }
+    int run = (t == 0) ? 0 : part[t - 1];
+    for (int i = beg; i < end; ++i) { ptr[i] = run; run += cnt[i]; }
+    if (t == 255) ptr[n] = part[255];
+  }
+  g.sync();
+
+  for (int i = gtid; i < ESS + EBIP + ESP; i += gsz) {
+    int p = (i >> 8) & 7;
+    if (i < ESS) {
+      int d = A.ss_col[i];
+      int pos = A.ss_ptr[d] + A.ss_cp[p * NSPAT + d] + A.ss_rnk[i];
+      A.ss_src[pos] = A.ss_row[i]; A.ss_cea[pos] = A.ss_eaI[i];
+    } else if (i < ESS + EBIP) {
+      int j = i - ESS;
+      int d = A.bp_col[j];
+      int pos = A.bp_ptr[d] + A.bp_cp[p * NSP + d] + A.bp_rnk[j];
+      A.bp_src[pos] = A.bp_row[j]; A.bp_cea[pos] = A.bp_eaI[j];
+    } else {
+      int j = i - ESS - EBIP;
+      int d = A.pp_col[j];
+      int pos = A.pp_ptr[d] + A.pp_cp[p * NSP + d] + A.pp_rnk[j];
+      A.pp_src[pos] = A.pp_row[j]; A.pp_cea[pos] = A.pp_eaI[j];
+    }
+  }
+  g.sync();
+
+  {
+    const int NB_LEAF = (NSPAT + NSP + 255) / 256;
+    const long totA = (long)NSP * 96, totB = (long)NSPAT * 16;
+    const int NB_PREP = (int)((totA + totB + 255) / 256);
+    const int NBT = NB_LEAF + 5 + NB_PREP;
+    int mode = *A.flag;
+    for (int b = blockIdx.x; b < NBT; b += gridDim.x) {
+      if (b < NB_LEAF) {
+        int i = b * 256 + t;
+        if (i < NSPAT + NSP) {
+          const int* ptr; const float* cea; float* lea; int d;
+          if (i < NSPAT) { ptr = A.ss_ptr; cea = A.ss_cea; lea = A.ss_lea; d = i; }
+          else { ptr = A.pp_ptr; cea = A.pp_cea; lea = A.pp_lea; d = i - NSPAT; }
+          int e0 = ptr[d], e1 = ptr[d + 1];
+          float s = 0.f;
+          for (int e = e0; e < e1; ++e) s += cea[e];
+          lea[d] = s / (float)max(e1 - e0, 1);
+        }
+      } else if (b < NB_LEAF + 5) {
+        int lb = b - NB_LEAF;
+        int n = (lb == 2) ? 64 : 256;
+        int off2 = lb * 4;
+        if (t < n) {
+          float p = wave_red_sum(A.We[lb][t] * A.ae[lb][t]);
+          if ((t & 63) == 0) A.dotes[off2 + (t >> 6)] = p;
+        }
+      } else {
+        long i = (long)(b - NB_LEAF - 5) * 256 + t;
+        if (i < totA + totB) {
+          if (i < totA) {
+            int n = (int)(i / 96), c = (int)(i % 96);
+            float v;
+            if (c < 32) v = A.mean[(long)n * 32 + c];
+            else if (c < 64) v = A.stdv[(long)n * 32 + (c - 32)];
+            else {
+              long j = (long)n * 32 + (c - 64);
+              int mv;
+              if (mode == 0) mv = ((const int*)A.mask)[j];
+              else if (mode == 2) mv = (((const float*)A.mask)[j] != 0.0f);
+              else mv = (int)((const unsigned char*)A.mask)[j];
+              v = mv ? 0.f : 1.f;
+            }
+            A.spc96[i] = v;
+          } else {
+            long k = i - totA;
+            int n = (int)(k / 16), c = (int)(k % 16);
+            A.h0[k] = (c < 12) ? A.sx[(long)n * 12 + c] : A.sgd[(long)n * 4 + (c - 12)];
+          }
+        }
+      }
+    }
+  }
+  g.sync();
+
+  proj64_grid(A.sl, wl, xl);
+  proj64_grid(A.bpWd, wl, xl);
+  g.sync();
+
+  proj256_grid(A.sg0, wl, xl);
+  g.sync();
+  gat4_grid(NSPAT, A.ss_ptr, A.ss_src, A.ss_cea, A.alS, A.alD, A.dotes + 0, A.ss_lea,
+            A.HS, A.sg0_b, A.h_a);
+  g.sync();
+  proj256_grid(A.sg1, wl, xl);
+  g.sync();
+  gat4_grid(NSPAT, A.ss_ptr, A.ss_src, A.ss_cea, A.alS, A.alD, A.dotes + 4, A.ss_lea,
+            A.HS, A.sg1_b, A.h_b);
+  g.sync();
+  proj64_grid(A.bpWs, wl, xl);
+  g.sync();
+  gat1_grid(NSP, A.bp_ptr, A.bp_src, A.bp_cea, A.alSb, A.alDb, A.dotes + 8,
+            A.h_a, A.bp_b, A.sts);
+  g.sync();
+  proj256_grid(A.pg0, wl, xl);
+  g.sync();
+  gat4_grid(NSP, A.pp_ptr, A.pp_src, A.pp_cea, A.alS, A.alD, A.dotes + 12, A.pp_lea,
+            A.HS, A.pg0_b, A.x1);
+  g.sync();
+  proj256_grid(A.pg1, wl, xl);
+  g.sync();
+  gat4_grid(NSP, A.pp_ptr, A.pp_src, A.pp_cea, A.alS, A.alD, A.dotes + 16, A.pp_lea,
+            A.HS, A.pg1_b, A.sts);
+  g.sync();
+  proj64_grid(A.fc, wl, xl);
 }
 
 extern "C" void kernel_launch(void* const* d_in, const int* in_sizes, int n_in,
@@ -648,87 +666,86 @@
   float* pp_lea = (float*)A((size_t)NSP * 4);
   (void)ws_size; (void)in_sizes; (void)n_in; (void)out_size;
 
-  const int TB = 256;
-  hipMemsetAsync(wsb, 0, zbytes, stream);
-
-  count3_kernel<<<cdiv_host(ESS + EBIP + ESP, TB) + 1, TB, 0, stream>>>(
-      ss_ei + ESS, ESS, ss_cp, ss_rnk, NSPAT,
-      bip_ei + EBIP, EBIP, bp_cp, bp_rnk, NSP,
-      sp_ei + ESP, ESP, pp_cp, pp_rnk, NSP,
-      (const unsigned int*)nanmask, flag);
-  merge3_kernel<<<cdiv_host(NSPAT + NSP + NSP, TB), TB, 0, stream>>>(
-      ss_cp, ss_cnt, NSPAT, bp_cp, bp_cnt, NSP, pp_cp, pp_cnt, NSP);
-  scan3_kernel<<<3, 1024, 0, stream>>>(ss_cnt, NSPAT, ss_ptr, bp_cnt, NSP, bp_ptr, pp_cnt, NSP, pp_ptr);
-  scatter3_kernel<<<cdiv_host(ESS + EBIP + ESP, TB), TB, 0, stream>>>(
-      ss_ei, ss_ei + ESS, ss_ea, ESS, ss_ptr, ss_cp, ss_rnk, NSPAT, ss_src, ss_cea,
-      bip_ei, bip_ei + EBIP, bip_ea, EBIP, bp_ptr, bp_cp, bp_rnk, NSP, bp_src, bp_cea,
-      sp_ei, sp_ei + ESP, sp_ea, ESP, pp_ptr, pp_cp, pp_rnk, NSP, pp_src, pp_cea);
-
-  misc_kernel<<<123 + cdiv_host((long)NSP * 96 + (long)NSPAT * 16, TB), TB, 0, stream>>>(
-      ss_ptr, ss_cea, ss_lea, pp_ptr, pp_cea, pp_lea,
-      sg0_We, sg0_ae, sg1_We, sg1_ae, bp_We, bp_ae, pg0_We, pg0_ae, pg1_We, pg1_ae,
-      dotes, sp_mean, sp_std, nanmask, flag, spat_x, spat_g, spc96, h0);
-
-  {
-    PJob j0{}; j0.xs.p[0] = spc96; j0.xs.w[0] = 96; j0.xs.p[1] = sp_gen; j0.xs.w[1] = 64;
-    j0.xs.p[2] = sp_phy; j0.xs.w[2] = 128; j0.xs.n = 3;
-    j0.M = NSP; j0.K = 288; j0.W = sl_W; j0.bias = sl_b; j0.mode = 1; j0.Y = sp_in;
-    PJob j1{}; j1.xs.p[0] = sp_gen; j1.xs.w[0] = 64; j1.xs.p[1] = sp_phy; j1.xs.w[1] = 128;
-    j1.xs.n = 2;
-    j1.M = NSP; j1.K = 192; j1.W = bp_Wd; j1.mode = 0; j1.a_d = bp_ad; j1.al_d = alDb;
-    int nb0 = cdiv_host(NSP, 32);
-    proj64x2_kernel<<<nb0 + cdiv_host(NSP, 32), TB, 0, stream>>>(j0, j1, nb0);
-  }
-
-  {
-    XSrc xs{}; xs.p[0] = h0; xs.w[0] = 16; xs.n = 1;
-    proj_kernel<<<cdiv_host(NSPAT, 32), TB, 0, stream>>>(xs, NSPAT, 16, sg0_W, nullptr, 3,
-        sg0_as, sg0_ad, alS, alD, HS, nullptr);
-  }
-  gat4_fused<true><<<cdiv_host(NSPAT, 4), TB, 0, stream>>>(
-      NSPAT, ss_ptr, ss_src, ss_cea, alS, alD, dotes + 0, ss_lea,
-      (const unsigned short*)HS, sg0_b, h_a);
-  {
-    XSrc xs{}; xs.p[0] = h_a; xs.w[0] = 64; xs.n = 1;
-    proj_kernel<<<cdiv_host(NSPAT, 32), TB, 0, stream>>>(xs, NSPAT, 64, sg1_W, nullptr, 3,
-        sg1_as, sg1_ad, alS, alD, HS, nullptr);
-  }
-  gat4_fused<true><<<cdiv_host(NSPAT, 4), TB, 0, stream>>>(
-      NSPAT, ss_ptr, ss_src, ss_cea, alS, alD, dotes + 4, ss_lea,
-      (const unsigned short*)HS, sg1_b, h_b);
-
-  {
-    PJob j0{}; j0.xs.p[0] = h_b; j0.xs.w[0] = 64; j0.xs.n = 1;
-    j0.M = NSPAT; j0.K = 64; j0.W = bp_Ws; j0.mode = 0;
-    j0.a_s = bp_as; j0.al_s = alSb; j0.Y = h_a;
-    int nb0 = cdiv_host(NSPAT, 32);
-    proj64x2_kernel<<<nb0, TB, 0, stream>>>(j0, j0, nb0);
-  }
-  gat1_fused<<<cdiv_host(NSP, 4), TB, 0, stream>>>(
-      NSP, bp_ptr, bp_src, bp_cea, alSb, alDb, dotes + 8, h_a, bp_b, sts);
-
-  {
-    XSrc xs{}; xs.p[0] = sts; xs.w[0] = 64; xs.p[1] = sp_in; xs.w[1] = 64; xs.n = 2;
-    proj_kernel<<<cdiv_host(NSP, 32), TB, 0, stream>>>(xs, NSP, 128, pg0_W, nullptr, 3,
-        pg0_as, pg0_ad, alS, alD, HS, nullptr);
-  }
-  gat4_fused<true><<<cdiv_host(NSP, 4), TB, 0, stream>>>(
-      NSP, pp_ptr, pp_src, pp_cea, alS, alD, dotes + 12, pp_lea,
-      (const unsigned short*)HS, pg0_b, x1);
-  {
-    XSrc xs{}; xs.p[0] = x1; xs.w[0] = 64; xs.n = 1;
-    proj_kernel<<<cdiv_host(NSP, 32), TB, 0, stream>>>(xs, NSP, 64, pg1_W, nullptr, 3,
-        pg1_as, pg1_ad, alS, alD, HS, nullptr);
-  }
-  gat4_fused<true><<<cdiv_host(NSP, 4), TB, 0, stream>>>(
-      NSP, pp_ptr, pp_src, pp_cea, alS, alD, dotes + 16, pp_lea,
-      (const unsigned short*)HS, pg1_b, sts);
-
-  {
-    PJob j0{}; j0.xs.p[0] = sts; j0.xs.w[0] = 64; j0.xs.n = 1;
-    j0.M = NSP; j0.K = 64; j0.W = fc_W; j0.bias = fc_b; j0.mode = 2;
-    j0.Y = (float*)d_out; j0.Y2 = (float*)d_out + (long)NSP * 32;
-    int nb0 = cdiv_host(NSP, 32);
-    proj64x2_kernel<<<nb0, TB, 0, stream>>>(j0, j0, nb0);
-  }
-}
+  MegaArgs ma{};
+  ma.zbase = (uint4*)wsb; ma.zwords = (int)(zbytes / 16);
+  ma.ss_row = ss_ei; ma.ss_col = ss_ei + ESS; ma.ss_eaI = ss_ea;
+  ma.bp_row = bip_ei; ma.bp_col = bip_ei + EBIP; ma.bp_eaI = bip_ea;
+  ma.pp_row = sp_ei; ma.pp_col = sp_ei + ESP; ma.pp_eaI = sp_ea;
+  ma.ss_cp = ss_cp; ma.bp_cp = bp_cp; ma.pp_cp = pp_cp;
+  ma.ss_rnk = ss_rnk; ma.bp_rnk = bp_rnk; ma.pp_rnk = pp_rnk;
+  ma.ss_cnt = ss_cnt; ma.bp_cnt = bp_cnt; ma.pp_cnt = pp_cnt;
+  ma.ss_ptr = ss_ptr; ma.bp_ptr = bp_ptr; ma.pp_ptr = pp_ptr;
+  ma.ss_src = ss_src; ma.ss_cea = ss_cea;
+  ma.bp_src = bp_src; ma.bp_cea = bp_cea;
+  ma.pp_src = pp_src; ma.pp_cea = pp_cea;
+  ma.ss_lea = ss_lea; ma.pp_lea = pp_lea;
+  ma.mask = (const unsigned int*)nanmask; ma.flag = flag;
+  ma.We[0] = sg0_We; ma.ae[0] = sg0_ae;
+  ma.We[1] = sg1_We; ma.ae[1] = sg1_ae;
+  ma.We[2] = bp_We;  ma.ae[2] = bp_ae;
+  ma.We[3] = pg0_We; ma.ae[3] = pg0_ae;
+  ma.We[4] = pg1_We; ma.ae[4] = pg1_ae;
+  ma.dotes = dotes;
+  ma.mean = sp_mean; ma.stdv = sp_std; ma.sx = spat_x; ma.sgd = spat_g;
+  ma.spc96 = spc96; ma.h0 = h0;
+
+  ma.sl.xs.p[0] = spc96; ma.sl.xs.w[0] = 96;
+  ma.sl.xs.p[1] = sp_gen; ma.sl.xs.w[1] = 64;
+  ma.sl.xs.p[2] = sp_phy; ma.sl.xs.w[2] = 128; ma.sl.xs.n = 3;
+  ma.sl.M = NSP; ma.sl.K = 288; ma.sl.W = sl_W; ma.sl.bias = sl_b;
+  ma.sl.mode = 1; ma.sl.Y = sp_in;
+
+  ma.bpWd.xs.p[0] = sp_gen; ma.bpWd.xs.w[0] = 64;
+  ma.bpWd.xs.p[1] = sp_phy; ma.bpWd.xs.w[1] = 128; ma.bpWd.xs.n = 2;
+  ma.bpWd.M = NSP; ma.bpWd.K = 192; ma.bpWd.W = bp_Wd; ma.bpWd.mode = 0;
+  ma.bpWd.a_d = bp_ad; ma.bpWd.al_d = alDb;
+
+  ma.bpWs.xs.p[0] = h_b; ma.bpWs.xs.w[0] = 64; ma.bpWs.xs.n = 1;
+  ma.bpWs.M = NSPAT; ma.bpWs.K = 64; ma.bpWs.W = bp_Ws; ma.bpWs.mode = 0;
+  ma.bpWs.a_s = bp_as; ma.bpWs.al_s = alSb; ma.bpWs.Y = h_a;
+
+  ma.fc.xs.p[0] = sts; ma.fc.xs.w[0] = 64; ma.fc.xs.n = 1;
+  ma.fc.M = NSP; ma.fc.K = 64; ma.fc.W = fc_W; ma.fc.bias = fc_b; ma.fc.mode = 2;
+  ma.fc.Y = (float*)d_out; ma.fc.Y2 = (float*)d_out + (long)NSP * 32;
+
+  ma.sg0.xs.p[0] = h0; ma.sg0.xs.w[0] = 16; ma.sg0.xs.n = 1;
+  ma.sg0.M = NSPAT; ma.sg0.K = 16; ma.sg0.W = sg0_W;
+  ma.sg0.a_s = sg0_as; ma.sg0.a_d = sg0_ad; ma.sg0.al_s = alS; ma.sg0.al_d = alD;
+  ma.sg0.Y = (unsigned short*)HS;
+
+  ma.sg1.xs.p[0] = h_a; ma.sg1.xs.w[0] = 64; ma.sg1.xs.n = 1;
+  ma.sg1.M = NSPAT; ma.sg1.K = 64; ma.sg1.W = sg1_W;
+  ma.sg1.a_s = sg1_as; ma.sg1.a_d = sg1_ad; ma.sg1.al_s = alS; ma.sg1.al_d = alD;
+  ma.sg1.Y = (unsigned short*)HS;
+
+  ma.pg0.xs.p[0] = sts; ma.pg0.xs.w[0] = 64;
+  ma.pg0.xs.p[1] = sp_in; ma.pg0.xs.w[1] = 64; ma.pg0.xs.n = 2;
+  ma.pg0.M = NSP; ma.pg0.K = 128; ma.pg0.W = pg0_W;
+  ma.pg0.a_s = pg0_as; ma.pg0.a_d = pg0_ad; ma.pg0.al_s = alS; ma.pg0.al_d = alD;
+  ma.pg0.Y = (unsigned short*)HS;
+
+  ma.pg1.xs.p[0] = x1; ma.pg1.xs.w[0] = 64; ma.pg1.xs.n = 1;
+  ma.pg1.M = NSP; ma.pg1.K = 64; ma.pg1.W = pg1_W;
+  ma.pg1.a_s = pg1_as; ma.pg1.a_d = pg1_ad; ma.pg1.al_s = alS; ma.pg1.al_d = alD;
+  ma.pg1.Y = (unsigned short*)HS;
+
+  ma.alS = alS; ma.alD = alD; ma.alSb = alSb; ma.alDb = alDb;
+  ma.HS = (const unsigned short*)HS;
+  ma.sg0_b = sg0_b; ma.sg1_b = sg1_b; ma.pg0_b = pg0_b; ma.pg1_b = pg1_b; ma.bp_b = bp_b;
+  ma.h_a = h_a; ma.h_b = h_b; ma.sts = sts; ma.x1 = x1;
+
+  int dev = 0;
+  hipGetDevice(&dev);
+  int numCU = 256;
+  hipDeviceGetAttribute(&numCU, hipDeviceAttributeMultiprocessorCount, dev);
+  int maxBpc = 0;
+  hipOccupancyMaxActiveBlocksPerMultiprocessor(&maxBpc, (const void*)mega_kernel, 256, 0);
+  if (maxBpc < 1) maxBpc = 1;
+  long grid = (long)maxBpc * numCU;
+  if (grid > 5000) grid = 5000;
+  if (grid < 3) grid = 3;
+
+  void* params[] = { &ma };
+  hipLaunchCooperativeKernel((const void*)mega_kernel, dim3((unsigned)grid), dim3(256),
+                             params, 0, stream);
+}
```

After: 1.676 ms. 236% more time.
